# Kernel optimization log

Measured on AMD Instinct MI355X. Metric: run time of the kernel, lower is better.

Reference implementation:

```python
import jax, jax.numpy as jnp
import numpy as np

N = 100000   # num_nodes
D = 128      # input_dim
DO = 128     # output_dim
V = 3        # num_views/relations
E = 500000   # edges per view
C = 2        # num_classes
H = D // 2   # label-attention hidden
VH = DO // 2 # view-attention hidden
EPS = 1e-5


def setup_inputs() -> dict:
    key = jax.random.key(0)
    ks = jax.random.split(key, 20)
    s = 0.05
    def nrm(k, shape):
        return jax.random.normal(k, shape, dtype=jnp.float32) * s
    return {
        'features': jax.random.normal(ks[0], (N, D), dtype=jnp.float32),
        'edge_src': jax.random.randint(ks[1], (V, E), 0, N, dtype=jnp.int32),
        'edge_dst': jax.random.randint(ks[2], (V, E), 0, N, dtype=jnp.int32),
        'edge_w': jax.random.uniform(ks[3], (V, E), dtype=jnp.float32),
        'clsW': nrm(ks[4], (D, C)), 'clsb': jnp.zeros((C,), jnp.float32),
        'attW1': nrm(ks[5], (C, D, H)), 'attb1': jnp.zeros((C, H), jnp.float32),
        'attW2': nrm(ks[6], (C, H)), 'attb2': jnp.zeros((C,), jnp.float32),
        'att_bias': jnp.float32(0.1),
        'relW': nrm(ks[7], (V, D, DO)), 'relb': jnp.zeros((V, DO), jnp.float32),
        'gateW': nrm(ks[8], (V, DO, DO)), 'gateb': jnp.zeros((V, DO), jnp.float32),
        'view_pref': jax.random.normal(ks[9], (V, DO), dtype=jnp.float32),
        'vattW1': nrm(ks[10], (DO, VH)), 'vattb1': jnp.zeros((VH,), jnp.float32),
        'vattW2': nrm(ks[11], (VH,)), 'vattb2': jnp.float32(0.0),
        'selfW': nrm(ks[12], (D, DO)), 'selfb': jnp.zeros((DO,), jnp.float32),
        'featW': nrm(ks[13], (D, DO)), 'featb': jnp.zeros((DO,), jnp.float32),
        'fusW': nrm(ks[14], (2 * DO, DO)), 'fusb': jnp.zeros((DO,), jnp.float32),
        'ln_g': jnp.ones((DO,), jnp.float32), 'ln_b': jnp.zeros((DO,), jnp.float32),
    }


def reference(features, edge_src, edge_dst, edge_w,
              clsW, clsb, attW1, attb1, attW2, attb2, att_bias,
              relW, relb, gateW, gateb,
              view_pref, vattW1, vattb1, vattW2, vattb2,
              selfW, selfb, featW, featb, fusW, fusb, ln_g, ln_b):
    # --- LabelAwareAttention ---
    class_probs = jax.nn.softmax(features @ clsW + clsb, axis=-1)          # [N,C]
    h = jax.nn.relu(jnp.einsum('nd,cdh->cnh', features, attW1) + attb1[:, None, :])
    scores = jax.nn.sigmoid(jnp.einsum('cnh,ch->cn', h, attW2) + attb2[:, None])
    node_att = jnp.sum(scores.T * class_probs, axis=-1) + att_bias         # [N]

    # --- per-view RelationAggregator (num_relations=1 -> relation weight is 1) ---
    src_f = features[edge_src]                                             # [V,E,D]
    msg = (jnp.einsum('ved,vdo->veo', src_f, relW) + relb[:, None, :]) \
          * edge_w[..., None]                                              # [V,E,DO]
    agg = jax.vmap(lambda m, d: jax.ops.segment_sum(m, d, num_segments=N))(
        msg, edge_dst)                                                     # [V,N,DO]
    gate = jax.nn.sigmoid(jnp.einsum('vno,vop->vnp', agg, gateW) + gateb[:, None, :])
    view_out = gate * agg                                                  # [V,N,DO]

    # --- ViewLevelAttention ---
    vh = jax.nn.relu(jnp.einsum('vno,oh->vnh', view_out * view_pref[:, None, :], vattW1) + vattb1)
    vscores = jnp.einsum('vnh,h->vn', vh, vattW2) + vattb2                 # [V,N]
    vweights = jax.nn.softmax(vscores, axis=0)                             # softmax over views
    combined = jnp.sum(view_out * vweights[..., None], axis=0)             # [N,DO]

    # --- fusion + residual + layer norm (dropout=0, eval) ---
    self_out = features @ selfW + selfb
    transformed = features @ featW + featb
    weighted = combined * node_att[:, None]
    fused = jax.nn.relu(jnp.concatenate([self_out, weighted], axis=-1) @ fusW + fusb)
    out = fused + transformed
    mu = jnp.mean(out, axis=-1, keepdims=True)
    var = jnp.var(out, axis=-1, keepdims=True)
    out = (out - mu) / jnp.sqrt(var + EPS) * ln_g + ln_b
    return out, class_probs
```

## Files before the change

### kernel.cpp

```cpp
#include <hip/hip_runtime.h>
#include <hip/hip_bf16.h>

#define NN 100000
#define DD 128
#define VV 3
#define EE 500000
#define TOT (VV * NN)
#define NB ((TOT + 255) / 256)
#define RGB ((NN + 127) / 128)

typedef unsigned short u16;
typedef unsigned int u32;
typedef short s8v __attribute__((ext_vector_type(8)));
typedef float f4v __attribute__((ext_vector_type(4)));

__device__ __forceinline__ float bf2f(u16 u) {
    return __uint_as_float(((u32)u) << 16);
}
__device__ __forceinline__ u16 f2bf(float f) {
    u32 x = __float_as_uint(f);
    u32 r = (x + 0x7fffu + ((x >> 16) & 1u)) >> 16;
    return (u16)r;
}

__device__ __forceinline__ float fexp2(float x) {
#if __has_builtin(__builtin_amdgcn_exp2f)
    return __builtin_amdgcn_exp2f(x);
#else
    return exp2f(x);
#endif
}
__device__ __forceinline__ float frcp(float x) {
#if __has_builtin(__builtin_amdgcn_rcpf)
    return __builtin_amdgcn_rcpf(x);
#else
    return 1.f / x;
#endif
}
__device__ __forceinline__ float fsigmoid(float x) {
    return frcp(1.f + fexp2(-1.4426950408889634f * x));
}

__device__ __forceinline__ void atomAddBf16x2(u16* addr, float f0, float f1) {
#if __has_builtin(__builtin_amdgcn_global_atomic_fadd_v2bf16)
    typedef short v2s __attribute__((ext_vector_type(2)));
    typedef v2s __attribute__((address_space(1)))* v2s_gp;
    v2s v;
    v.x = (short)f2bf(f0);
    v.y = (short)f2bf(f1);
    __builtin_amdgcn_global_atomic_fadd_v2bf16((v2s_gp)(void*)addr, v);
#else
    u32* p = (u32*)addr;
    u32 old = *(volatile u32*)p;
    while (true) {
        float lo = bf2f((u16)(old & 0xffffu)) + f0;
        float hi = bf2f((u16)(old >> 16)) + f1;
        u32 nv = (u32)f2bf(lo) | ((u32)f2bf(hi) << 16);
        u32 prev = atomicCAS(p, old, nv);
        if (prev == old) break;
        old = prev;
    }
#endif
}

template<int XSTR, int WSTR>
__device__ __forceinline__ void gemm16(float acc[4][4], const float* Xs,
                                       const float* Ws, int n0, int o0, int kbase) {
    #pragma unroll 4
    for (int kk = 0; kk < 64; kk += 4) {
        float4 w0 = *reinterpret_cast<const float4*>(Ws + (kk + 0) * WSTR + o0);
        float4 w1 = *reinterpret_cast<const float4*>(Ws + (kk + 1) * WSTR + o0);
        float4 w2 = *reinterpret_cast<const float4*>(Ws + (kk + 2) * WSTR + o0);
        float4 w3 = *reinterpret_cast<const float4*>(Ws + (kk + 3) * WSTR + o0);
        #pragma unroll
        for (int i = 0; i < 4; ++i) {
            float4 x = *reinterpret_cast<const float4*>(Xs + (n0 + i) * XSTR + kbase + kk);
            acc[i][0] = fmaf(x.x, w0.x, fmaf(x.y, w1.x, fmaf(x.z, w2.x, fmaf(x.w, w3.x, acc[i][0]))));
            acc[i][1] = fmaf(x.x, w0.y, fmaf(x.y, w1.y, fmaf(x.z, w2.y, fmaf(x.w, w3.y, acc[i][1]))));
            acc[i][2] = fmaf(x.x, w0.z, fmaf(x.y, w1.z, fmaf(x.z, w2.z, fmaf(x.w, w3.z, acc[i][2]))));
            acc[i][3] = fmaf(x.x, w0.w, fmaf(x.y, w1.w, fmaf(x.z, w2.w, fmaf(x.w, w3.w, acc[i][3]))));
        }
    }
}

template<int WSTR, int NT>
__device__ __forceinline__ void stage_w_f32(float* Ws, const float* __restrict__ src, int tid) {
    #pragma unroll
    for (int rep = 0; rep < 2048 / NT; ++rep) {
        int flat = rep * NT + tid;
        int kk = flat >> 5;
        int c4 = flat & 31;
        float4 q = *reinterpret_cast<const float4*>(src + kk * 128 + c4 * 4);
        *reinterpret_cast<float4*>(Ws + kk * WSTR + c4 * 4) = q;
    }
}

template<int XSTR, int NT>
__device__ __forceinline__ void stage_x_f32(float* Xs, const float* __restrict__ src, int tid) {
    #pragma unroll
    for (int rep = 0; rep < 1024 / NT; ++rep) {
        int flat = rep * NT + tid;
        int n = flat >> 5;
        int c4 = flat & 31;
        float4 q = *reinterpret_cast<const float4*>(src + (size_t)n * 128 + c4 * 4);
        *reinterpret_cast<float4*>(Xs + n * XSTR + c4 * 4) = q;
    }
}

template<int XSTR, int NT>
__device__ __forceinline__ void stage_x_bf16(float* Xs, const u16* __restrict__ src, int tid) {
    #pragma unroll
    for (int rep = 0; rep < 512 / NT; ++rep) {
        int flat = rep * NT + tid;
        int n = flat >> 4;
        int c8 = flat & 15;
        uint4 q = *reinterpret_cast<const uint4*>(src + (size_t)n * 128 + c8 * 8);
        float* d = Xs + n * XSTR + c8 * 8;
        d[0] = bf2f((u16)(q.x & 0xffffu)); d[1] = bf2f((u16)(q.x >> 16));
        d[2] = bf2f((u16)(q.y & 0xffffu)); d[3] = bf2f((u16)(q.y >> 16));
        d[4] = bf2f((u16)(q.z & 0xffffu)); d[5] = bf2f((u16)(q.z >> 16));
        d[6] = bf2f((u16)(q.w & 0xffffu)); d[7] = bf2f((u16)(q.w >> 16));
    }
}

__global__ void prep_kernel(const float* __restrict__ selfW, const float* __restrict__ selfb,
                            const float* __restrict__ fusW, const float* __restrict__ fusb,
                            float* __restrict__ Wsf, float* __restrict__ c1) {
    int o = threadIdx.x;
    int k = blockIdx.x;
    if (k < 128) {
        float acc = 0.f;
        for (int m = 0; m < 128; ++m)
            acc += selfW[k * 128 + m] * fusW[m * 128 + o];
        Wsf[k * 128 + o] = acc;
    } else {
        float acc = 0.f;
        for (int m = 0; m < 128; ++m)
            acc += selfb[m] * fusW[m * 128 + o];
        c1[o] = acc + fusb[o];
    }
}

__global__ __launch_bounds__(128) void wprep_kernel(
        const float* __restrict__ relW, const float* __restrict__ gateW,
        u16* __restrict__ relWb, u16* __restrict__ gateWb) {
    int k = threadIdx.x;
    int n = blockIdx.x & 127;
    int v = blockIdx.x >> 7;
    size_t o = ((size_t)v * 128 + n) * 128 + k;
    size_t i = ((size_t)v * 128 + k) * 128 + n;
    relWb[o]  = f2bf(relW[i]);
    gateWb[o] = f2bf(gateW[i]);
}

__global__ __launch_bounds__(128) void wprep2_kernel(
        const float* __restrict__ Wsf, const float* __restrict__ featW,
        const float* __restrict__ fusW,
        u16* __restrict__ WsfB, u16* __restrict__ featWB, u16* __restrict__ fusWbB) {
    int k = threadIdx.x;
    int n = blockIdx.x;
    WsfB[n * 128 + k]   = f2bf(Wsf[k * 128 + n]);
    featWB[n * 128 + k] = f2bf(featW[k * 128 + n]);
    fusWbB[n * 128 + k] = f2bf(fusW[(size_t)(128 + k) * 128 + n]);
}

__global__ __launch_bounds__(128) void wprep3_kernel(
        const float* __restrict__ attW1, u16* __restrict__ attW1B) {
    int k = threadIdx.x;
    int o = blockIdx.x;
    int c = o >> 6, h = o & 63;
    attW1B[o * 128 + k] = f2bf(attW1[((size_t)c * 128 + k) * 64 + h]);
}

__global__ __launch_bounds__(128) void wprep4_kernel(
        const float* __restrict__ vattW1, const float* __restrict__ view_pref,
        u16* __restrict__ vattW1p) {
    int k = threadIdx.x;
    int h = blockIdx.x & 63;
    int v = blockIdx.x >> 6;
    vattW1p[((size_t)v * 64 + h) * 128 + k] =
        f2bf(view_pref[v * 128 + k] * vattW1[k * 64 + h]);
}

__global__ __launch_bounds__(128) void wprep5_kernel(
        const float* __restrict__ relW, const float* __restrict__ gateW,
        const float* __restrict__ relb,
        u16* __restrict__ W12b, float* __restrict__ rgb) {
    int p = threadIdx.x;
    int b = blockIdx.x;
    int v = b / 129;
    int d = b - v * 129;
    const float* gW = gateW + (size_t)v * 128 * 128;
    if (d < 128) {
        const float* rW = relW + ((size_t)v * 128 + d) * 128;
        float acc = 0.f;
        for (int o = 0; o < 128; ++o) acc += rW[o] * gW[o * 128 + p];
        W12b[((size_t)v * 128 + p) * 128 + d] = f2bf(acc);
    } else {
        const float* rb = relb + (size_t)v * 128;
        float acc = 0.f;
        for (int o = 0; o < 128; ++o) acc += rb[o] * gW[o * 128 + p];
        rgb[v * 128 + p] = acc;
    }
}

__global__ __launch_bounds__(256) void featconv_kernel(
        const float* __restrict__ feat, u16* __restrict__ featB) {
    int t = blockIdx.x * 256 + threadIdx.x;
    float4 q = *reinterpret_cast<const float4*>(feat + (size_t)t * 4);
    ushort4 r;
    r.x = f2bf(q.x); r.y = f2bf(q.y); r.z = f2bf(q.z); r.w = f2bf(q.w);
    *reinterpret_cast<ushort4*>(featB + (size_t)t * 4) = r;
}


__global__ __launch_bounds__(256) void count_kernel(
        const int* __restrict__ edst, int* __restrict__ C) {
    int t = blockIdx.x * 256 + threadIdx.x;
    if (t >= VV * EE) return;
    int v = t / EE;
    atomicAdd(&C[v * NN + edst[t]], 1);
}

__global__ __launch_bounds__(256) void scanA_kernel(
        const int* __restrict__ C, int* __restrict__ bs) {
    int b = blockIdx.x, t = threadIdx.x;
    int i = b * 256 + t;
    int v = (i < TOT) ? C[i] : 0;
    __shared__ int s[256];
    s[t] = v;
    __syncthreads();
    #pragma unroll
    for (int off = 128; off > 0; off >>= 1) {
        if (t < off) s[t] += s[t + off];
        __syncthreads();
    }
    if (t == 0) bs[b] = s[0];
}

__global__ __launch_bounds__(1024) void scanB_kernel(int* __restrict__ bs) {
    __shared__ int s[2048];
    int t = threadIdx.x;
    int v0 = (t < NB) ? bs[t] : 0;
    int v1 = (t + 1024 < NB) ? bs[t + 1024] : 0;
    s[t] = v0; s[t + 1024] = v1;
    __syncthreads();
    #pragma unroll
    for (int off = 1; off < 2048; off <<= 1) {
        int x0 = (t >= off) ? s[t - off] : 0;
        int x1 = (t + 1024 >= off) ? s[t + 1024 - off] : 0;
        __syncthreads();
        s[t] += x0; s[t + 1024] += x1;
        __syncthreads();
    }
    if (t < NB) bs[t] = s[t] - v0;
    if (t + 1024 < NB) bs[t + 1024] = s[t + 1024] - v1;
}

__global__ __launch_bounds__(256) void scanC_kernel(
        int* __restrict__ C, const int* __restrict__ bs) {
    int b = blockIdx.x, t = threadIdx.x;
    int i = b * 256 + t;
    int v = (i < TOT) ? C[i] : 0;
    __shared__ int s[256];
    s[t] = v;
    __syncthreads();
    #pragma unroll
    for (int off = 1; off < 256; off <<= 1) {
        int x = (t >= off) ? s[t - off] : 0;
        __syncthreads();
        s[t] += x;
        __syncthreads();
    }
    if (i < TOT) C[i] = s[t] - v + bs[b];
}

__global__ __launch_bounds__(256) void fill_kernel(
        const int* __restrict__ esrc, const int* __restrict__ edst,
        const float* __restrict__ ew, int* __restrict__ C,
        int2* __restrict__ bsw) {
    int t = blockIdx.x * 256 + threadIdx.x;
    if (t >= VV * EE) return;
    int v = t / EE;
    int pos = atomicAdd(&C[v * NN + edst[t]], 1);
    int2 p;
    p.x = esrc[t];
    p.y = __float_as_int(ew[t]);
    bsw[pos] = p;
}

__global__ __launch_bounds__(256) void gather_kernel(
        const u16* __restrict__ featB, const int* __restrict__ C,
        const int2* __restrict__ bsw,
        u16* __restrict__ aggB, float* __restrict__ wsum) {
    int wid = (blockIdx.x * 256 + threadIdx.x) >> 6;
    int lane = threadIdx.x & 63;
    int end = C[wid];
    int start = (wid == 0) ? 0 : C[wid - 1];
    float a0 = 0.f, a1 = 0.f, wacc = 0.f;
    int e = start;
    for (; e + 4 <= end; e += 4) {
        int2 p0 = bsw[e], p1 = bsw[e + 1], p2 = bsw[e + 2], p3 = bsw[e + 3];
        u32 f0 = *reinterpret_cast<const u32*>(featB + (size_t)p0.x * DD + lane * 2);
        u32 f1 = *reinterpret_cast<const u32*>(featB + (size_t)p1.x * DD + lane * 2);
        u32 f2 = *reinterpret_cast<const u32*>(featB + (size_t)p2.x * DD + lane * 2);
        u32 f3 = *reinterpret_cast<const u32*>(featB + (size_t)p3.x * DD + lane * 2);
        float w0 = __int_as_float(p0.y), w1 = __int_as_float(p1.y);
        float w2 = __int_as_float(p2.y), w3 = __int_as_float(p3.y);
        a0 = fmaf(w0, bf2f((u16)(f0 & 0xffffu)), a0);
        a1 = fmaf(w0, bf2f((u16)(f0 >> 16)), a1);
        a0 = fmaf(w1, bf2f((u16)(f1 & 0xffffu)), a0);
        a1 = fmaf(w1, bf2f((u16)(f1 >> 16)), a1);
        a0 = fmaf(w2, bf2f((u16)(f2 & 0xffffu)), a0);
        a1 = fmaf(w2, bf2f((u16)(f2 >> 16)), a1);
        a0 = fmaf(w3, bf2f((u16)(f3 & 0xffffu)), a0);
        a1 = fmaf(w3, bf2f((u16)(f3 >> 16)), a1);
        wacc += (w0 + w1) + (w2 + w3);
    }
    for (; e < end; ++e) {
        int2 p = bsw[e];
        float w = __int_as_float(p.y);
        u32 f = *reinterpret_cast<const u32*>(featB + (size_t)p.x * DD + lane * 2);
        a0 = fmaf(w, bf2f((u16)(f & 0xffffu)), a0);
        a1 = fmaf(w, bf2f((u16)(f >> 16)), a1);
        wacc += w;
    }
    u32 packed = (u32)f2bf(a0) | ((u32)f2bf(a1) << 16);
    *reinterpret_cast<u32*>(aggB + (size_t)wid * DD + lane * 2) = packed;
    if (lane == 0) wsum[wid] = wacc;
}

__global__ __launch_bounds__(256) void scatter_kernel(
        const int* __restrict__ esrc, const int* __restrict__ edst,
        const float* __restrict__ ew, const float* __restrict__ feat,
        u16* __restrict__ aggB, float* __restrict__ wsum) {
    long long t = (long long)blockIdx.x * 256 + threadIdx.x;
    int lane = (int)(t & 31);
    int eg = (int)(t >> 5);
    int v = eg / EE;
    int src = 0, dst = 0; float w = 0.f;
    if (lane == 0) {
        src = esrc[eg]; dst = edst[eg]; w = ew[eg];
    }
    src = __shfl(src, 0, 32);
    dst = __shfl(dst, 0, 32);
    w   = __shfl(w, 0, 32);
    const float* fr = feat + (size_t)src * DD + lane * 4;
    float4 q = *reinterpret_cast<const float4*>(fr);
    u16* outp = aggB + ((size_t)v * NN + dst) * DD + lane * 4;
    atomAddBf16x2(outp,     w * q.x, w * q.y);
    atomAddBf16x2(outp + 2, w * q.z, w * q.w);
    if (lane == 0) atomicAdd(wsum + v * NN + dst, w);
}

__global__ __launch_bounds__(256) void label_mfma_kernel(
        const u16* __restrict__ featB, const u16* __restrict__ attW1B,
        const float* __restrict__ clsW, const float* __restrict__ clsb,
        const float* __restrict__ attb1, const float* __restrict__ attW2,
        const float* __restrict__ attb2, const float* __restrict__ att_bias,
        float* __restrict__ node_att, float* __restrict__ probs_out) {
    __shared__ u16 Xs[128][136];
    __shared__ u16 Wt[128][72];
    int tid = threadIdx.x;
    int wv = tid >> 6, lane = tid & 63;
    int quad = lane >> 4, l15 = lane & 15;
    int row0 = blockIdx.x * 128;

    #pragma unroll
    for (int rep = 0; rep < 8; ++rep) {
        int flat = rep * 256 + tid;
        int n = flat >> 4, c8 = flat & 15;
        int gr = row0 + n; if (gr >= NN) gr = NN - 1;
        uint4 q = *reinterpret_cast<const uint4*>(featB + (size_t)gr * DD + c8 * 8);
        *reinterpret_cast<uint4*>(&Xs[n][c8 * 8]) = q;
    }

    f4v acc[2][8];
    #pragma unroll
    for (int rt = 0; rt < 2; ++rt)
        #pragma unroll
        for (int c = 0; c < 8; ++c)
            acc[rt][c] = f4v{0.f, 0.f, 0.f, 0.f};

    #pragma unroll
    for (int h = 0; h < 2; ++h) {
        #pragma unroll
        for (int rep = 0; rep < 4; ++rep) {
            int flat = rep * 256 + tid;
            int n = flat >> 3, c8 = flat & 7;
            uint4 q = *reinterpret_cast<const uint4*>(attW1B + (size_t)n * DD + h * 64 + c8 * 8);
            *reinterpret_cast<uint4*>(&Wt[n][c8 * 8]) = q;
        }
        __syncthreads();
        #pragma unroll
        for (int t = 0; t < 2; ++t) {
            int kl = t * 32 + quad * 8;
            s8v a0 = *reinterpret_cast<const s8v*>(&Xs[wv * 32 + l15][h * 64 + kl]);
            s8v a1 = *reinterpret_cast<const s8v*>(&Xs[wv * 32 + 16 + l15][h * 64 + kl]);
            #pragma unroll
            for (int c = 0; c < 8; ++c) {
                s8v b = *reinterpret_cast<const s8v*>(&Wt[c * 16 + l15][kl]);
                acc[0][c] = __builtin_amdgcn_mfma_f32_16x16x32_bf16(a0, b, acc[0][c], 0, 0, 0);
                acc[1][c] = __builtin_amdgcn_mfma_f32_16x16x32_bf16(a1, b, acc[1][c], 0, 0, 0);
            }
        }
        __syncthreads();
    }

    float ab1[8], aw2[8];
    #pragma unroll
    for (int c = 0; c < 8; ++c) {
        int col = c * 16 + l15;
        ab1[c] = attb1[col];
        aw2[c] = attW2[col];
    }
    float cw0[8], cw1[8];
    #pragma unroll
    for (int j = 0; j < 8; ++j) {
        int k = l15 * 8 + j;
        cw0[j] = clsW[k * 2];
        cw1[j] = clsW[k * 2 + 1];
    }
    float cb0 = clsb[0], cb1 = clsb[1];
    float b20 = attb2[0], b21 = attb2[1];
    float abias = att_bias[0];

    #pragma unroll
    for (int rt = 0; rt < 2; ++rt)
        #pragma unroll
        for (int r = 0; r < 4; ++r) {
            int n = wv * 32 + rt * 16 + quad * 4 + r;
            int gr = row0 + n;
            float p0 = 0.f, p1 = 0.f;
            #pragma unroll
            for (int c = 0; c < 4; ++c) {
                float hv = acc[rt][c][r] + ab1[c];
                hv = hv > 0.f ? hv : 0.f;
                p0 += hv * aw2[c];
            }
            #pragma unroll
            for (int c = 4; c < 8; ++c) {
                float hv = acc[rt][c][r] + ab1[c];
                hv = hv > 0.f ? hv : 0.f;
                p1 += hv * aw2[c];
            }
            uint4 q = *reinterpret_cast<const uint4*>(&Xs[n][l15 * 8]);
            float f[8];
            f[0] = bf2f((u16)(q.x & 0xffffu)); f[1] = bf2f((u16)(q.x >> 16));
            f[2] = bf2f((u16)(q.y & 0xffffu)); f[3] = bf2f((u16)(q.y >> 16));
            f[4] = bf2f((u16)(q.z & 0xffffu)); f[5] = bf2f((u16)(q.z >> 16));
            f[6] = bf2f((u16)(q.w & 0xffffu)); f[7] = bf2f((u16)(q.w >> 16));
            float l0 = 0.f, l1 = 0.f;
            #pragma unroll
            for (int j = 0; j < 8; ++j) {
                l0 = fmaf(f[j], cw0[j], l0);
                l1 = fmaf(f[j], cw1[j], l1);
            }
            #pragma unroll
            for (int m = 1; m < 16; m <<= 1) {
                p0 += __shfl_xor(p0, m);
                p1 += __shfl_xor(p1, m);
                l0 += __shfl_xor(l0, m);
                l1 += __shfl_xor(l1, m);
            }
            if (l15 == 0 && gr < NN) {
                float s0 = 1.f / (1.f + expf(-(p0 + b20)));
                float s1 = 1.f / (1.f + expf(-(p1 + b21)));
                l0 += cb0; l1 += cb1;
                float mm = fmaxf(l0, l1);
                float e0 = expf(l0 - mm), e1 = expf(l1 - mm);
                float inv = 1.f / (e0 + e1);
                float q0 = e0 * inv, q1 = e1 * inv;
                node_att[gr] = q0 * s0 + q1 * s1 + abias;
                probs_out[gr * 2]     = q0;
                probs_out[gr * 2 + 1] = q1;
            }
        }
}

__global__ __launch_bounds__(256) void label_kernel(
        const float* __restrict__ feat, const float* __restrict__ clsW, const float* __restrict__ clsb,
        const float* __restrict__ attW1, const float* __restrict__ attb1,
        const float* __restrict__ attW2, const float* __restrict__ attb2,
        const float* __restrict__ att_bias,
        float* __restrict__ node_att, float* __restrict__ probs_out) {
    __shared__ float Xs[32][132];
    __shared__ float Ws[64][132];
    int tid = threadIdx.x;
    int row0 = blockIdx.x * 32;
    stage_x_f32<132, 256>(&Xs[0][0], feat + (size_t)row0 * DD, tid);
    int to = tid & 31, tn = tid >> 5;
    int o0 = to * 4, n0 = tn * 4;
    float acc[4][4] = {};
    for (int half = 0; half < 2; ++half) {
        __syncthreads();
        #pragma unroll
        for (int rep = 0; rep < 8; ++rep) {
            int flat = rep * 256 + tid;
            int kk = flat >> 5, o4 = flat & 31;
            int o = o4 * 4;
            int c = o >> 6, h = o & 63;
            int k = half * 64 + kk;
            float4 q = *reinterpret_cast<const float4*>(attW1 + (size_t)(c * 128 + k) * 64 + h);
            *reinterpret_cast<float4*>(&Ws[kk][o]) = q;
        }
        __syncthreads();
        gemm16<132, 132>(acc, &Xs[0][0], &Ws[0][0], n0, o0, half * 64);
    }
    int c = o0 >> 6, h0 = o0 & 63;
    float b1j[4], w2j[4];
    #pragma unroll
    for (int j = 0; j < 4; ++j) {
        b1j[j] = attb1[c * 64 + h0 + j];
        w2j[j] = attW2[c * 64 + h0 + j];
    }
    float part[4];
    #pragma unroll
    for (int i = 0; i < 4; ++i) {
        float s = 0.f;
        #pragma unroll
        for (int j = 0; j < 4; ++j) {
            float hv = acc[i][j] + b1j[j];
            hv = hv > 0.f ? hv : 0.f;
            s += hv * w2j[j];
        }
        part[i] = s;
    }
    __syncthreads();
    float* red = &Ws[0][0];
    float* Ssc = red + 32 * 33;
    float* Lsc = Ssc + 64;
    #pragma unroll
    for (int i = 0; i < 4; ++i) red[(n0 + i) * 33 + to] = part[i];
    __syncthreads();
    if (tid < 64) {
        int n = tid >> 1, cc = tid & 1;
        float l = 0.f;
        for (int k = 0; k < 128; k += 4) {
            float4 x = *reinterpret_cast<const float4*>(&Xs[n][k]);
            l += x.x * clsW[(k + 0) * 2 + cc];
            l += x.y * clsW[(k + 1) * 2 + cc];
            l += x.z * clsW[(k + 2) * 2 + cc];
            l += x.w * clsW[(k + 3) * 2 + cc];
        }
        Lsc[n * 2 + cc] = l + clsb[cc];
        float s = 0.f;
        for (int u = 0; u < 16; ++u) s += red[n * 33 + cc * 16 + u];
        s += attb2[cc];
        Ssc[n * 2 + cc] = 1.f / (1.f + expf(-s));
    }
    __syncthreads();
    if (tid < 32) {
        int n = tid;
        float l0 = Lsc[n * 2], l1 = Lsc[n * 2 + 1];
        float m = fmaxf(l0, l1);
        float e0 = expf(l0 - m), e1 = expf(l1 - m);
        float inv = 1.f / (e0 + e1);
        float p0 = e0 * inv, p1 = e1 * inv;
        float na = p0 * Ssc[n * 2] + p1 * Ssc[n * 2 + 1] + att_bias[0];
        int row = row0 + n;
        node_att[row] = na;
        probs_out[row * 2]     = p0;
        probs_out[row * 2 + 1] = p1;
    }
}

__global__ __launch_bounds__(256, 3) void relgate_mfma_kernel(
        const u16* __restrict__ relWb, const float* __restrict__ relb,
        const u16* __restrict__ W12b, const float* __restrict__ rgb,
        const float* __restrict__ gateb,
        const u16* __restrict__ vattW1p, const float* __restrict__ vattb1,
        const float* __restrict__ vattW2, const float* __restrict__ vattb2,
        u16* __restrict__ aggB, const float* __restrict__ wsum,
        float* __restrict__ vscores) {
    __shared__ u16 Wf[128][136];
    __shared__ u16 Wt[128][72];
    int tid = threadIdx.x;
    int wv = tid >> 6, lane = tid & 63;
    int quad = lane >> 4, l15 = lane & 15;
    int v = blockIdx.y;
    int row0 = blockIdx.x * 128;
    const size_t vbase = (size_t)v * NN;

    #pragma unroll
    for (int rep = 0; rep < 8; ++rep) {
        int flat = rep * 256 + tid;
        int n = flat >> 4, c8 = flat & 15;
        int gr = row0 + n; if (gr >= NN) gr = NN - 1;
        uint4 q = *reinterpret_cast<const uint4*>(aggB + (vbase + gr) * DD + c8 * 8);
        *reinterpret_cast<uint4*>(&Wf[n][c8 * 8]) = q;
    }
    __syncthreads();

    s8v af[2][2][2];
    #pragma unroll
    for (int h = 0; h < 2; ++h)
        #pragma unroll
        for (int t = 0; t < 2; ++t) {
            int kl = h * 64 + t * 32 + quad * 8;
            af[h][t][0] = *reinterpret_cast<const s8v*>(&Wf[wv * 32 + l15][kl]);
            af[h][t][1] = *reinterpret_cast<const s8v*>(&Wf[wv * 32 + 16 + l15][kl]);
        }
    __syncthreads();

    const u16* W1 = relWb + (size_t)v * DD * DD;
    const u16* W2 = W12b + (size_t)v * DD * DD;
    #pragma unroll
    for (int rep = 0; rep < 8; ++rep) {
        int flat = rep * 256 + tid;
        int n = flat >> 4, c8 = flat & 15;
        *reinterpret_cast<uint4*>(&Wf[n][c8 * 8]) =
            *reinterpret_cast<const uint4*>(W1 + (size_t)n * DD + c8 * 8);
    }
    #pragma unroll
    for (int rep = 0; rep < 4; ++rep) {
        int flat = rep * 256 + tid;
        int n = flat >> 3, c8 = flat & 7;
        *reinterpret_cast<uint4*>(&Wt[n][c8 * 8]) =
            *reinterpret_cast<const uint4*>(W2 + (size_t)n * DD + c8 * 8);
    }
    __syncthreads();

    f4v acc1[2][8], acc2[2][8];
    #pragma unroll
    for (int rt = 0; rt < 2; ++rt)
        #pragma unroll
        for (int c = 0; c < 8; ++c) {
            acc1[rt][c] = f4v{0.f, 0.f, 0.f, 0.f};
            acc2[rt][c] = f4v{0.f, 0.f, 0.f, 0.f};
        }

    #pragma unroll
    for (int h = 0; h < 2; ++h)
        #pragma unroll
        for (int t = 0; t < 2; ++t) {
            int kl = h * 64 + t * 32 + quad * 8;
            #pragma unroll
            for (int c = 0; c < 8; ++c) {
                s8v b = *reinterpret_cast<const s8v*>(&Wf[c * 16 + l15][kl]);
                acc1[0][c] = __builtin_amdgcn_mfma_f32_16x16x32_bf16(af[h][t][0], b, acc1[0][c], 0, 0, 0);
                acc1[1][c] = __builtin_amdgcn_mfma_f32_16x16x32_bf16(af[h][t][1], b, acc1[1][c], 0, 0, 0);
            }
        }
    #pragma unroll
    for (int t = 0; t < 2; ++t) {
        int kl = t * 32 + quad * 8;
        #pragma unroll
        for (int c = 0; c < 8; ++c) {
            s8v b = *reinterpret_cast<const s8v*>(&Wt[c * 16 + l15][kl]);
            acc2[0][c] = __builtin_amdgcn_mfma_f32_16x16x32_bf16(af[0][t][0], b, acc2[0][c], 0, 0, 0);
            acc2[1][c] = __builtin_amdgcn_mfma_f32_16x16x32_bf16(af[0][t][1], b, acc2[1][c], 0, 0, 0);
        }
    }
    __syncthreads();

    #pragma unroll
    for (int rep = 0; rep < 4; ++rep) {
        int flat = rep * 256 + tid;
        int n = flat >> 3, c8 = flat & 7;
        *reinterpret_cast<uint4*>(&Wt[n][c8 * 8]) =
            *reinterpret_cast<const uint4*>(W2 + (size_t)n * DD + 64 + c8 * 8);
    }
    __syncthreads();
    #pragma unroll
    for (int t = 0; t < 2; ++t) {
        int kl = t * 32 + quad * 8;
        #pragma unroll
        for (int c = 0; c < 8; ++c) {
            s8v b = *reinterpret_cast<const s8v*>(&Wt[c * 16 + l15][kl]);
            acc2[0][c] = __builtin_amdgcn_mfma_f32_16x16x32_bf16(af[1][t][0], b, acc2[0][c], 0, 0, 0);
            acc2[1][c] = __builtin_amdgcn_mfma_f32_16x16x32_bf16(af[1][t][1], b, acc2[1][c], 0, 0, 0);
        }
    }

    float wsn[2][4];
    #pragma unroll
    for (int rt = 0; rt < 2; ++rt)
        #pragma unroll
        for (int r = 0; r < 4; ++r) {
            int gr = row0 + wv * 32 + rt * 16 + quad * 4 + r;
            wsn[rt][r] = wsum[vbase + (gr < NN ? gr : NN - 1)];
        }
    float rb[8], rg2[8], gb[8];
    #pragma unroll
    for (int c = 0; c < 8; ++c) {
        int col = c * 16 + l15;
        rb[c]  = relb[v * DD + col];
        rg2[c] = rgb[v * DD + col];
        gb[c]  = gateb[v * DD + col];
    }
    #pragma unroll
    for (int rt = 0; rt < 2; ++rt)
        #pragma unroll
        for (int c = 0; c < 8; ++c)
            #pragma unroll
            for (int r = 0; r < 4; ++r) {
                float a = acc1[rt][c][r] + wsn[rt][r] * rb[c];
                float g = fsigmoid(acc2[rt][c][r] + wsn[rt][r] * rg2[c] + gb[c]);
                Wf[wv * 32 + rt * 16 + quad * 4 + r][c * 16 + l15] = f2bf(g * a);
            }
    __syncthreads();

    {
        const u16* Wv = vattW1p + (size_t)v * 64 * DD;
        #pragma unroll
        for (int rep = 0; rep < 4; ++rep) {
            int flat = rep * 256 + tid;
            int n = flat >> 4, c8 = flat & 15;
            uint4 q = *reinterpret_cast<const uint4*>(Wv + (size_t)n * DD + c8 * 8);
            int half = c8 >> 3;
            *reinterpret_cast<uint4*>(&Wt[half * 64 + n][(c8 & 7) * 8]) = q;
        }
    }
    s8v a2[2][2][2];
    #pragma unroll
    for (int h = 0; h < 2; ++h)
        #pragma unroll
        for (int t = 0; t < 2; ++t) {
            int kl = h * 64 + t * 32 + quad * 8;
            a2[h][t][0] = *reinterpret_cast<const s8v*>(&Wf[wv * 32 + l15][kl]);
            a2[h][t][1] = *reinterpret_cast<const s8v*>(&Wf[wv * 32 + 16 + l15][kl]);
        }
    #pragma unroll
    for (int rep = 0; rep < 8; ++rep) {
        int flat = rep * 256 + tid;
        int n = flat >> 4, c8 = flat & 15;
        int gr = row0 + n;
        if (gr < NN)
            *reinterpret_cast<uint4*>(aggB + (vbase + gr) * DD + c8 * 8) =
                *reinterpret_cast<const uint4*>(&Wf[n][c8 * 8]);
    }
    __syncthreads();

    f4v acc3[2][4];
    #pragma unroll
    for (int rt = 0; rt < 2; ++rt)
        #pragma unroll
        for (int c = 0; c < 4; ++c)
            acc3[rt][c] = f4v{0.f, 0.f, 0.f, 0.f};
    #pragma unroll
    for (int h = 0; h < 2; ++h)
        #pragma unroll
        for (int t = 0; t < 2; ++t) {
            int kl = t * 32 + quad * 8;
            #pragma unroll
            for (int c = 0; c < 4; ++c) {
                s8v b = *reinterpret_cast<const s8v*>(&Wt[h * 64 + c * 16 + l15][kl]);
                acc3[0][c] = __builtin_amdgcn_mfma_f32_16x16x32_bf16(a2[h][t][0], b, acc3[0][c], 0, 0, 0);
                acc3[1][c] = __builtin_amdgcn_mfma_f32_16x16x32_bf16(a2[h][t][1], b, acc3[1][c], 0, 0, 0);
            }
        }
    float vb1[4], vw2[4];
    #pragma unroll
    for (int c = 0; c < 4; ++c) {
        int col = c * 16 + l15;
        vb1[c] = vattb1[col];
        vw2[c] = vattW2[col];
    }
    float vb2 = vattb2[0];
    #pragma unroll
    for (int rt = 0; rt < 2; ++rt)
        #pragma unroll
        for (int r = 0; r < 4; ++r) {
            float p = 0.f;
            #pragma unroll
            for (int c = 0; c < 4; ++c) {
                float hv = acc3[rt][c][r] + vb1[c];
                hv = hv > 0.f ? hv : 0.f;
                p += hv * vw2[c];
            }
            #pragma unroll
            for (int m = 1; m < 16; m <<= 1)
                p += __shfl_xor(p, m);
            int gr = row0 + wv * 32 + rt * 16 + quad * 4 + r;
            if (l15 == 0 && gr < NN)
                vscores[vbase + gr] = p + vb2;
        }
}

__global__ __launch_bounds__(256) void relgate_kernel(
        const float* __restrict__ relW, const float* __restrict__ relb,
        const float* __restrict__ gateW, const float* __restrict__ gateb,
        u16* __restrict__ aggB, const float* __restrict__ wsum) {
    __shared__ float Xs[32][128];
    __shared__ float Ws[64][132];
    int tid = threadIdx.x;
    int v = blockIdx.y;
    int row0 = blockIdx.x * 32;
    u16* base = aggB + ((size_t)v * NN + row0) * DD;
    stage_x_bf16<128, 256>(&Xs[0][0], base, tid);
    int to = tid & 31, tn = tid >> 5;
    int o0 = to * 4, n0 = tn * 4;
    float acc[4][4] = {};
    const float* W1 = relW + (size_t)v * DD * DD;
    for (int half = 0; half < 2; ++half) {
        __syncthreads();
        stage_w_f32<132, 256>(&Ws[0][0], W1 + half * 64 * DD, tid);
        __syncthreads();
        gemm16<128, 132>(acc, &Xs[0][0], &Ws[0][0], n0, o0, half * 64);
    }
    float wsn[4], rb[4];
    #pragma unroll
    for (int i = 0; i < 4; ++i) wsn[i] = wsum[v * NN + row0 + n0 + i];
    #pragma unroll
    for (int j = 0; j < 4; ++j) rb[j] = relb[v * DD + o0 + j];
    #pragma unroll
    for (int i = 0; i < 4; ++i)
        #pragma unroll
        for (int j = 0; j < 4; ++j) acc[i][j] += wsn[i] * rb[j];
    __syncthreads();
    #pragma unroll
    for (int i = 0; i < 4; ++i)
        *reinterpret_cast<float4*>(&Xs[n0 + i][o0]) = make_float4(acc[i][0], acc[i][1], acc[i][2], acc[i][3]);
    float acc2[4][4] = {};
    const float* W2 = gateW + (size_t)v * DD * DD;
    for (int half = 0; half < 2; ++half) {
        __syncthreads();
        stage_w_f32<132, 256>(&Ws[0][0], W2 + half * 64 * DD, tid);
        __syncthreads();
        gemm16<128, 132>(acc2, &Xs[0][0], &Ws[0][0], n0, o0, half * 64);
    }
    float gb[4];
    #pragma unroll
    for (int j = 0; j < 4; ++j) gb[j] = gateb[v * DD + o0 + j];
    #pragma unroll
    for (int i = 0; i < 4; ++i) {
        float g0 = 1.f / (1.f + expf(-(acc2[i][0] + gb[0])));
        float g1 = 1.f / (1.f + expf(-(acc2[i][1] + gb[1])));
        float g2 = 1.f / (1.f + expf(-(acc2[i][2] + gb[2])));
        float g3 = 1.f / (1.f + expf(-(acc2[i][3] + gb[3])));
        ushort4 r;
        r.x = f2bf(g0 * acc[i][0]); r.y = f2bf(g1 * acc[i][1]);
        r.z = f2bf(g2 * acc[i][2]); r.w = f2bf(g3 * acc[i][3]);
        *reinterpret_cast<ushort4*>(base + (size_t)(n0 + i) * DD + o0) = r;
    }
}

__global__ __launch_bounds__(128) void vatt_kernel(
        const u16* __restrict__ aggB, const float* __restrict__ view_pref,
        const float* __restrict__ vattW1, const float* __restrict__ vattb1,
        const float* __restrict__ vattW2, const float* __restrict__ vattb2,
        float* __restrict__ vscores) {
    __shared__ float Xs[32][132];
    __shared__ float Ws[128][68];
    int tid = threadIdx.x;
    int v = blockIdx.y;
    int row0 = blockIdx.x * 32;
    const u16* base = aggB + ((size_t)v * NN + row0) * DD;
    #pragma unroll
    for (int rep = 0; rep < 4; ++rep) {
        int flat = rep * 128 + tid;
        int n = flat >> 4, c8 = flat & 15;
        uint4 q = *reinterpret_cast<const uint4*>(base + (size_t)n * DD + c8 * 8);
        float4 pa = *reinterpret_cast<const float4*>(view_pref + v * DD + c8 * 8);
        float4 pb = *reinterpret_cast<const float4*>(view_pref + v * DD + c8 * 8 + 4);
        float* d = &Xs[n][c8 * 8];
        d[0] = bf2f((u16)(q.x & 0xffffu)) * pa.x; d[1] = bf2f((u16)(q.x >> 16)) * pa.y;
        d[2] = bf2f((u16)(q.y & 0xffffu)) * pa.z; d[3] = bf2f((u16)(q.y >> 16)) * pa.w;
        d[4] = bf2f((u16)(q.z & 0xffffu)) * pb.x; d[5] = bf2f((u16)(q.z >> 16)) * pb.y;
        d[6] = bf2f((u16)(q.w & 0xffffu)) * pb.z; d[7] = bf2f((u16)(q.w >> 16)) * pb.w;
    }
    #pragma unroll
    for (int rep = 0; rep < 16; ++rep) {
        int flat = rep * 128 + tid;
        int k = flat >> 4, c4 = flat & 15;
        float4 q = *reinterpret_cast<const float4*>(vattW1 + k * 64 + c4 * 4);
        *reinterpret_cast<float4*>(&Ws[k][c4 * 4]) = q;
    }
    __syncthreads();
    int to = tid & 15, tn = tid >> 4;
    int o0 = to * 4, n0 = tn * 4;
    float acc[4][4] = {};
    gemm16<132, 68>(acc, &Xs[0][0], &Ws[0][0], n0, o0, 0);
    gemm16<132, 68>(acc, &Xs[0][0], &Ws[64][0], n0, o0, 64);
    float b1[4], w2[4];
    #pragma unroll
    for (int j = 0; j < 4; ++j) {
        b1[j] = vattb1[o0 + j];
        w2[j] = vattW2[o0 + j];
    }
    float part[4];
    #pragma unroll
    for (int i = 0; i < 4; ++i) {
        float s = 0.f;
        #pragma unroll
        for (int j = 0; j < 4; ++j) {
            float hv = acc[i][j] + b1[j];
            hv = hv > 0.f ? hv : 0.f;
            s += hv * w2[j];
        }
        part[i] = s;
    }
    __syncthreads();
    float* red = &Ws[0][0];
    #pragma unroll
    for (int i = 0; i < 4; ++i) red[(n0 + i) * 17 + to] = part[i];
    __syncthreads();
    if (tid < 32) {
        float s = 0.f;
        for (int u = 0; u < 16; ++u) s += red[tid * 17 + u];
        vscores[(size_t)v * NN + row0 + tid] = s + vattb2[0];
    }
}

__global__ __launch_bounds__(256) void combine_kernel(
        u16* __restrict__ aggB, const float* __restrict__ vscores,
        const float* __restrict__ node_att) {
    int t = blockIdx.x * 256 + threadIdx.x;
    int n = t >> 5, c4 = t & 31;
    float s0 = vscores[n], s1 = vscores[NN + n], s2 = vscores[2 * NN + n];
    float m = fmaxf(s0, fmaxf(s1, s2));
    float e0 = expf(s0 - m), e1 = expf(s1 - m), e2 = expf(s2 - m);
    float inv = 1.f / (e0 + e1 + e2);
    float w0 = e0 * inv, w1 = e1 * inv, w2 = e2 * inv;
    float na = node_att[n];
    size_t off = (size_t)n * DD + c4 * 4;
    ushort4 q0 = *reinterpret_cast<const ushort4*>(aggB + off);
    ushort4 q1 = *reinterpret_cast<const ushort4*>(aggB + (size_t)NN * DD + off);
    ushort4 q2 = *reinterpret_cast<const ushort4*>(aggB + 2 * (size_t)NN * DD + off);
    ushort4 r;
    r.x = f2bf((bf2f(q0.x) * w0 + bf2f(q1.x) * w1 + bf2f(q2.x) * w2) * na);
    r.y = f2bf((bf2f(q0.y) * w0 + bf2f(q1.y) * w1 + bf2f(q2.y) * w2) * na);
    r.z = f2bf((bf2f(q0.z) * w0 + bf2f(q1.z) * w1 + bf2f(q2.z) * w2) * na);
    r.w = f2bf((bf2f(q0.w) * w0 + bf2f(q1.w) * w1 + bf2f(q2.w) * w2) * na);
    *reinterpret_cast<ushort4*>(aggB + off) = r;
}

__global__ __launch_bounds__(256, 3) void final_mfma_kernel(
        const u16* __restrict__ featB, const u16* __restrict__ aggB,
        const float* __restrict__ vsc, const float* __restrict__ natt,
        const u16* __restrict__ WsfB, const u16* __restrict__ featWB,
        const u16* __restrict__ fusWbB,
        const float* __restrict__ c1, const float* __restrict__ featb,
        const float* __restrict__ ln_g, const float* __restrict__ ln_b,
        float* __restrict__ outp) {
    __shared__ u16 Wf[128][136];
    __shared__ u16 Wt[128][72];
    int tid = threadIdx.x;
    int wv = tid >> 6, lane = tid & 63;
    int quad = lane >> 4, l15 = lane & 15;
    int row0 = blockIdx.x * 128;

    #pragma unroll
    for (int rep = 0; rep < 8; ++rep) {
        int flat = rep * 256 + tid;
        int n = flat >> 4, c8 = flat & 15;
        int gr = row0 + n; if (gr >= NN) gr = NN - 1;
        uint4 q = *reinterpret_cast<const uint4*>(featB + (size_t)gr * DD + c8 * 8);
        *reinterpret_cast<uint4*>(&Wf[n][c8 * 8]) = q;
    }
    if (tid < 128) {
        int gr = row0 + tid; if (gr >= NN) gr = NN - 1;
        float s0 = vsc[gr], s1 = vsc[NN + gr], s2 = vsc[2 * NN + gr];
        float m = fmaxf(s0, fmaxf(s1, s2));
        const float L2E = 1.4426950408889634f;
        float e0 = fexp2((s0 - m) * L2E);
        float e1 = fexp2((s1 - m) * L2E);
        float e2 = fexp2((s2 - m) * L2E);
        float na = natt[gr] * frcp(e0 + e1 + e2);
        float* rwp = reinterpret_cast<float*>(&Wf[tid][128]);
        rwp[0] = e0 * na;
        rwp[1] = e1 * na;
        rwp[2] = e2 * na;
    }
    __syncthreads();

    s8v af[2][2][2];
    #pragma unroll
    for (int h = 0; h < 2; ++h)
        #pragma unroll
        for (int t = 0; t < 2; ++t) {
            int kl = h * 64 + t * 32 + quad * 8;
            af[h][t][0] = *reinterpret_cast<const s8v*>(&Wf[wv * 32 + l15][kl]);
            af[h][t][1] = *reinterpret_cast<const s8v*>(&Wf[wv * 32 + 16 + l15][kl]);
        }
    __syncthreads();

    #pragma unroll
    for (int rep = 0; rep < 8; ++rep) {
        int flat = rep * 256 + tid;
        int n = flat >> 4, c8 = flat & 15;
        *reinterpret_cast<uint4*>(&Wf[n][c8 * 8]) =
            *reinterpret_cast<const uint4*>(WsfB + (size_t)n * DD + c8 * 8);
    }
    #pragma unroll
    for (int rep = 0; rep < 4; ++rep) {
        int flat = rep * 256 + tid;
        int n = flat >> 3, c8 = flat & 7;
        *reinterpret_cast<uint4*>(&Wt[n][c8 * 8]) =
            *reinterpret_cast<const uint4*>(featWB + (size_t)n * DD + c8 * 8);
    }
    __syncthreads();

    f4v acc1[2][8], acc2[2][8];
    #pragma unroll
    for (int rt = 0; rt < 2; ++rt)
        #pragma unroll
        for (int c = 0; c < 8; ++c) {
            acc1[rt][c] = f4v{0.f, 0.f, 0.f, 0.f};
            acc2[rt][c] = f4v{0.f, 0.f, 0.f, 0.f};
        }

    #pragma unroll
    for (int h = 0; h < 2; ++h)
        #pragma unroll
        for (int t = 0; t < 2; ++t) {
            int kl = h * 64 + t * 32 + quad * 8;
            #pragma unroll
            for (int c = 0; c < 8; ++c) {
                s8v b = *reinterpret_cast<const s8v*>(&Wf[c * 16 + l15][kl]);
                acc1[0][c] = __builtin_amdgcn_mfma_f32_16x16x32_bf16(af[h][t][0], b, acc1[0][c], 0, 0, 0);
                acc1[1][c] = __builtin_amdgcn_mfma_f32_16x16x32_bf16(af[h][t][1], b, acc1[1][c], 0, 0, 0);
            }
        }
    #pragma unroll
    for (int t = 0; t < 2; ++t) {
        int kl = t * 32 + quad * 8;
        #pragma unroll
        for (int c = 0; c < 8; ++c) {
            s8v b = *reinterpret_cast<const s8v*>(&Wt[c * 16 + l15][kl]);
            acc2[0][c] = __builtin_amdgcn_mfma_f32_16x16x32_bf16(af[0][t][0], b, acc2[0][c], 0, 0, 0);
            acc2[1][c] = __builtin_amdgcn_mfma_f32_16x16x32_bf16(af[0][t][1], b, acc2[1][c], 0, 0, 0);
        }
    }
    __syncthreads();
    #pragma unroll
    for (int rep = 0; rep < 4; ++rep) {
        int flat = rep * 256 + tid;
        int n = flat >> 3, c8 = flat & 7;
        *reinterpret_cast<uint4*>(&Wt[n][c8 * 8]) =
            *reinterpret_cast<const uint4*>(featWB + (size_t)n * DD + 64 + c8 * 8);
    }
    __syncthreads();
    #pragma unroll
    for (int t = 0; t < 2; ++t) {
        int kl = t * 32 + quad * 8;
        #pragma unroll
        for (int c = 0; c < 8; ++c) {
            s8v b = *reinterpret_cast<const s8v*>(&Wt[c * 16 + l15][kl]);
            acc2[0][c] = __builtin_amdgcn_mfma_f32_16x16x32_bf16(af[1][t][0], b, acc2[0][c], 0, 0, 0);
            acc2[1][c] = __builtin_amdgcn_mfma_f32_16x16x32_bf16(af[1][t][1], b, acc2[1][c], 0, 0, 0);
        }
    }

    #pragma unroll
    for (int rep = 0; rep < 8; ++rep) {
        int flat = rep * 256 + tid;
        int n = flat >> 4, c8 = flat & 15;
        int gr = row0 + n; if (gr >= NN) gr = NN - 1;
        size_t off = (size_t)gr * DD + c8 * 8;
        uint4 q0 = *reinterpret_cast<const uint4*>(aggB + off);
        uint4 q1 = *reinterpret_cast<const uint4*>(aggB + (size_t)NN * DD + off);
        uint4 q2 = *reinterpret_cast<const uint4*>(aggB + 2 * (size_t)NN * DD + off);
        const float* rwp = reinterpret_cast<const float*>(&Wf[n][128]);
        float w0 = rwp[0], w1 = rwp[1], w2 = rwp[2];
        u32 o[4];
        const u32* a = &q0.x; const u32* b = &q1.x; const u32* c = &q2.x;
        #pragma unroll
        for (int j = 0; j < 4; ++j) {
            float lo = bf2f((u16)(a[j] & 0xffffu)) * w0 + bf2f((u16)(b[j] & 0xffffu)) * w1
                     + bf2f((u16)(c[j] & 0xffffu)) * w2;
            float hi = bf2f((u16)(a[j] >> 16)) * w0 + bf2f((u16)(b[j] >> 16)) * w1
                     + bf2f((u16)(c[j] >> 16)) * w2;
            o[j] = (u32)f2bf(lo) | ((u32)f2bf(hi) << 16);
        }
        uint4 r; r.x = o[0]; r.y = o[1]; r.z = o[2]; r.w = o[3];
        *reinterpret_cast<uint4*>(&Wf[n][c8 * 8]) = r;
    }
    __syncthreads();

    #pragma unroll
    for (int rep = 0; rep < 4; ++rep) {
        int flat = rep * 256 + tid;
        int n = flat >> 3, c8 = flat & 7;
        *reinterpret_cast<uint4*>(&Wt[n][c8 * 8]) =
            *reinterpret_cast<const uint4*>(fusWbB + (size_t)n * DD + c8 * 8);
    }
    __syncthreads();
    #pragma unroll
    for (int t = 0; t < 2; ++t) {
        int kl = t * 32 + quad * 8;
        s8v a0 = *reinterpret_cast<const s8v*>(&Wf[wv * 32 + l15][kl]);
        s8v a1 = *reinterpret_cast<const s8v*>(&Wf[wv * 32 + 16 + l15][kl]);
        #pragma unroll
        for (int c = 0; c < 8; ++c) {
            s8v b = *reinterpret_cast<const s8v*>(&Wt[c * 16 + l15][kl]);
            acc1[0][c] = __builtin_amdgcn_mfma_f32_16x16x32_bf16(a0, b, acc1[0][c], 0, 0, 0);
            acc1[1][c] = __builtin_amdgcn_mfma_f32_16x16x32_bf16(a1, b, acc1[1][c], 0, 0, 0);
        }
    }
    __syncthreads();
    #pragma unroll
    for (int rep = 0; rep < 4; ++rep) {
        int flat = rep * 256 + tid;
        int n = flat >> 3, c8 = flat & 7;
        *reinterpret_cast<uint4*>(&Wt[n][c8 * 8]) =
            *reinterpret_cast<const uint4*>(fusWbB + (size_t)n * DD + 64 + c8 * 8);
    }
    __syncthreads();
    #pragma unroll
    for (int t = 0; t < 2; ++t) {
        int kl = t * 32 + quad * 8;
        s8v a0 = *reinterpret_cast<const s8v*>(&Wf[wv * 32 + l15][64 + kl]);
        s8v a1 = *reinterpret_cast<const s8v*>(&Wf[wv * 32 + 16 + l15][64 + kl]);
        #pragma unroll
        for (int c = 0; c < 8; ++c) {
            s8v b = *reinterpret_cast<const s8v*>(&Wt[c * 16 + l15][kl]);
            acc1[0][c] = __builtin_amdgcn_mfma_f32_16x16x32_bf16(a0, b, acc1[0][c], 0, 0, 0);
            acc1[1][c] = __builtin_amdgcn_mfma_f32_16x16x32_bf16(a1, b, acc1[1][c], 0, 0, 0);
        }
    }

    float c1j[8], fbj[8], gj[8], bj[8];
    #pragma unroll
    for (int c = 0; c < 8; ++c) {
        int col = c * 16 + l15;
        c1j[c] = c1[col];
        fbj[c] = featb[col];
        gj[c]  = ln_g[col];
        bj[c]  = ln_b[col];
    }
    #pragma unroll
    for (int rt = 0; rt < 2; ++rt)
        #pragma unroll
        for (int c = 0; c < 8; ++c)
            #pragma unroll
            for (int r = 0; r < 4; ++r) {
                float f = acc1[rt][c][r] + c1j[c];
                f = f > 0.f ? f : 0.f;
                acc1[rt][c][r] = f + acc2[rt][c][r] + fbj[c];
            }
    #pragma unroll
    for (int rt = 0; rt < 2; ++rt)
        #pragma unroll
        for (int r = 0; r < 4; ++r) {
            float s = 0.f, q = 0.f;
            #pragma unroll
            for (int c = 0; c < 8; ++c) {
                float x = acc1[rt][c][r];
                s += x; q += x * x;
            }
            #pragma unroll
            for (int m = 1; m < 16; m <<= 1) {
                s += __shfl_xor(s, m);
                q += __shfl_xor(q, m);
            }
            float mu = s * (1.f / 128.f);
            float var = q * (1.f / 128.f) - mu * mu;
            float rs = rsqrtf(var + 1e-5f);
            int gr = row0 + wv * 32 + rt * 16 + quad * 4 + r;
            if (gr < NN) {
                #pragma unroll
                for (int c = 0; c < 8; ++c)
                    outp[(size_t)gr * DD + c * 16 + l15] =
                        (acc1[rt][c][r] - mu) * rs * gj[c] + bj[c];
            }
        }
}

__global__ __launch_bounds__(256) void final_kernel(
        const float* __restrict__ feat, const u16* __restrict__ weightedB,
        const float* __restrict__ Wsf, const float* __restrict__ c1,
        const float* __restrict__ fusW, const float* __restrict__ featW,
        const float* __restrict__ featb, const float* __restrict__ ln_g,
        const float* __restrict__ ln_b, float* __restrict__ outp) {
    __shared__ float Xs[32][128];
    __shared__ float Ws[64][128];
    int tid = threadIdx.x;
    int row0 = blockIdx.x * 32;
    stage_x_f32<128, 256>(&Xs[0][0], feat + (size_t)row0 * DD, tid);
    int to = tid & 31, tn = tid >> 5;
    int o0 = to * 4, n0 = tn * 4;
    float acc1[4][4] = {}, acc2[4][4] = {};
    for (int half = 0; half < 2; ++half) {
        __syncthreads();
        stage_w_f32<128, 256>(&Ws[0][0], Wsf + half * 64 * 128, tid);
        __syncthreads();
        gemm16<128, 128>(acc1, &Xs[0][0], &Ws[0][0], n0, o0, half * 64);
    }
    for (int half = 0; half < 2; ++half) {
        __syncthreads();
        stage_w_f32<128, 256>(&Ws[0][0], featW + half * 64 * 128, tid);
        __syncthreads();
        gemm16<128, 128>(acc2, &Xs[0][0], &Ws[0][0], n0, o0, half * 64);
    }
    __syncthreads();
    stage_x_bf16<128, 256>(&Xs[0][0], weightedB + (size_t)row0 * DD, tid);
    for (int half = 0; half < 2; ++half) {
        __syncthreads();
        stage_w_f32<128, 256>(&Ws[0][0], fusW + (size_t)(128 + half * 64) * 128, tid);
        __syncthreads();
        gemm16<128, 128>(acc1, &Xs[0][0], &Ws[0][0], n0, o0, half * 64);
    }
    float c1j[4], fbj[4], gj[4], bj[4];
    #pragma unroll
    for (int j = 0; j < 4; ++j) {
        c1j[j] = c1[o0 + j];
        fbj[j] = featb[o0 + j];
        gj[j]  = ln_g[o0 + j];
        bj[j]  = ln_b[o0 + j];
    }
    float val[4][4];
    #pragma unroll
    for (int i = 0; i < 4; ++i)
        #pragma unroll
        for (int j = 0; j < 4; ++j) {
            float f = acc1[i][j] + c1j[j];
            f = f > 0.f ? f : 0.f;
            val[i][j] = f + acc2[i][j] + fbj[j];
        }
    __syncthreads();
    float* red_s = &Ws[0][0];
    float* red_q = red_s + 32 * 33;
    float* mus   = red_q + 32 * 33;
    float* rss   = mus + 32;
    #pragma unroll
    for (int i = 0; i < 4; ++i) {
        float s = 0.f, q = 0.f;
        #pragma unroll
        for (int j = 0; j < 4; ++j) { s += val[i][j]; q += val[i][j] * val[i][j]; }
        red_s[(n0 + i) * 33 + to] = s;
        red_q[(n0 + i) * 33 + to] = q;
    }
    __syncthreads();
    if (tid < 32) {
        float s = 0.f, q = 0.f;
        for (int u = 0; u < 32; ++u) { s += red_s[tid * 33 + u]; q += red_q[tid * 33 + u]; }
        float mu = s / 128.f;
        float var = q / 128.f - mu * mu;
        mus[tid] = mu;
        rss[tid] = rsqrtf(var + 1e-5f);
    }
    __syncthreads();
    #pragma unroll
    for (int i = 0; i < 4; ++i) {
        float mu = mus[n0 + i], rs = rss[n0 + i];
        float4 o;
        o.x = (val[i][0] - mu) * rs * gj[0] + bj[0];
        o.y = (val[i][1] - mu) * rs * gj[1] + bj[1];
        o.z = (val[i][2] - mu) * rs * gj[2] + bj[2];
        o.w = (val[i][3] - mu) * rs * gj[3] + bj[3];
        *reinterpret_cast<float4*>(outp + (size_t)(row0 + n0 + i) * DD + o0) = o;
    }
}

extern "C" void kernel_launch(void* const* d_in, const int* in_sizes, int n_in,
                              void* d_out, int out_size, void* d_ws, size_t ws_size,
                              hipStream_t stream) {
    (void)in_sizes; (void)n_in; (void)out_size;
    const float* feat      = (const float*)d_in[0];
    const int*   esrc      = (const int*)d_in[1];
    const int*   edst      = (const int*)d_in[2];
    const float* ew        = (const float*)d_in[3];
    const float* clsW      = (const float*)d_in[4];
    const float* clsb      = (const float*)d_in[5];
    const float* attW1     = (const float*)d_in[6];
    const float* attb1     = (const float*)d_in[7];
    const float* attW2     = (const float*)d_in[8];
    const float* attb2     = (const float*)d_in[9];
    const float* att_bias  = (const float*)d_in[10];
    const float* relW      = (const float*)d_in[11];
    const float* relb      = (const float*)d_in[12];
    const float* gateW     = (const float*)d_in[13];
    const float* gateb     = (const float*)d_in[14];
    const float* view_pref = (const float*)d_in[15];
    const float* vattW1    = (const float*)d_in[16];
    const float* vattb1    = (const float*)d_in[17];
    const float* vattW2    = (const float*)d_in[18];
    const float* vattb2    = (const float*)d_in[19];
    const float* selfW     = (const float*)d_in[20];
    const float* selfb     = (const float*)d_in[21];
    const float* featW     = (const float*)d_in[22];
    const float* featb     = (const float*)d_in[23];
    const float* fusW      = (const float*)d_in[24];
    const float* fusb      = (const float*)d_in[25];
    const float* ln_g      = (const float*)d_in[26];
    const float* ln_b      = (const float*)d_in[27];

    u16*   aggB = (u16*)d_ws;
    float* wsum = (float*)(aggB + (size_t)VV * NN * DD);
    float* natt = wsum + (size_t)VV * NN;
    float* vsc  = natt + NN;
    float* Wsf  = vsc + (size_t)VV * NN;
    float* c1   = Wsf + DD * DD;
    u16* relWb  = (u16*)(c1 + DD);
    u16* gateWb = relWb + (size_t)VV * DD * DD;
    u16* WsfB   = gateWb + (size_t)VV * DD * DD;
    u16* featWB = WsfB + DD * DD;
    u16* fusWbB = featWB + DD * DD;
    u16* attW1B = fusWbB + DD * DD;
    u16* vattW1p = attW1B + DD * DD;
    u16* W12b   = vattW1p + (size_t)VV * 64 * DD;
    float* rgb  = (float*)(W12b + (size_t)VV * DD * DD);
    int*   C    = (int*)(rgb + VV * DD);
    int*   bs   = C + (size_t)TOT;
    int2*  bsw  = (int2*)(bs + NB + 1);
    u16* featB  = (u16*)(bsw + (size_t)VV * EE);
    size_t needed = (size_t)((char*)(featB + (size_t)NN * DD) - (char*)d_ws);

    float* outp  = (float*)d_out;
    float* probs = outp + (size_t)NN * DD;

    prep_kernel<<<129, 128, 0, stream>>>(selfW, selfb, fusW, fusb, Wsf, c1);
    if (ws_size >= needed) {
        featconv_kernel<<<12500, 256, 0, stream>>>(feat, featB);
        wprep_kernel<<<384, 128, 0, stream>>>(relW, gateW, relWb, gateWb);
        wprep2_kernel<<<128, 128, 0, stream>>>(Wsf, featW, fusW, WsfB, featWB, fusWbB);
        wprep3_kernel<<<128, 128, 0, stream>>>(attW1, attW1B);
        wprep4_kernel<<<192, 128, 0, stream>>>(vattW1, view_pref, vattW1p);
        wprep5_kernel<<<VV * 129, 128, 0, stream>>>(relW, gateW, relb, W12b, rgb);
        label_mfma_kernel<<<RGB, 256, 0, stream>>>(featB, attW1B, clsW, clsb, attb1,
                                                   attW2, attb2, att_bias, natt, probs);
        hipMemsetAsync(C, 0, (size_t)TOT * sizeof(int), stream);
        count_kernel<<<(VV * EE + 255) / 256, 256, 0, stream>>>(edst, C);
        scanA_kernel<<<NB, 256, 0, stream>>>(C, bs);
        scanB_kernel<<<1, 1024, 0, stream>>>(bs);
        scanC_kernel<<<NB, 256, 0, stream>>>(C, bs);
        fill_kernel<<<(VV * EE + 255) / 256, 256, 0, stream>>>(esrc, edst, ew, C, bsw);
        gather_kernel<<<(VV * NN) / 4, 256, 0, stream>>>(featB, C, bsw, aggB, wsum);
        relgate_mfma_kernel<<<dim3(RGB, 3), 256, 0, stream>>>(relWb, relb, W12b, rgb, gateb,
                                                              vattW1p, vattb1, vattW2, vattb2,
                                                              aggB, wsum, vsc);
        final_mfma_kernel<<<RGB, 256, 0, stream>>>(featB, aggB, vsc, natt,
                                                   WsfB, featWB, fusWbB,
                                                   c1, featb, ln_g, ln_b, outp);
    } else {
        label_kernel<<<3125, 256, 0, stream>>>(feat, clsW, clsb, attW1, attb1, attW2, attb2,
                                               att_bias, natt, probs);
        hipMemsetAsync(d_ws, 0,
                       (size_t)VV * NN * DD * sizeof(u16) + (size_t)VV * NN * sizeof(float),
                       stream);
        scatter_kernel<<<187500, 256, 0, stream>>>(esrc, edst, ew, feat, aggB, wsum);
        relgate_kernel<<<dim3(3125, 3), 256, 0, stream>>>(relW, relb, gateW, gateb, aggB, wsum);
        vatt_kernel<<<dim3(3125, 3), 128, 0, stream>>>(aggB, view_pref, vattW1, vattb1,
                                                       vattW2, vattb2, vsc);
        combine_kernel<<<12500, 256, 0, stream>>>(aggB, vsc, natt);
        final_kernel<<<3125, 256, 0, stream>>>(feat, aggB, Wsf, c1, fusW, featW, featb,
                                               ln_g, ln_b, outp);
    }
}
```

Before: 661.3 us.

## Fuse label attention, relation/gate, view attention and final fusion into one kernel

Merges label_mfma, relgate_mfma and final_mfma into a single per-row-tile kernel. It loops over the three views while keeping view outputs and an online softmax over view scores in registers, then performs the fusion GEMMs and layer norm. This removes the intermediate global writes and re-reads of node_att, view scores and the per-view aggregates, plus two kernel launches. In exchange the single block carries many more accumulators, which raises register pressure and may lower occupancy. It also serializes the three views inside one block where they previously ran as a 3D grid.

```diff
diff --git a/kernel.cpp b/kernel.cpp
--- a/kernel.cpp
+++ b/kernel.cpp
@@ -121,6 +121,81 @@
         d[4] = bf2f((u16)(q.z & 0xffffu)); d[5] = bf2f((u16)(q.z >> 16));
         d[6] = bf2f((u16)(q.w & 0xffffu)); d[7] = bf2f((u16)(q.w >> 16));
     }
+}
+
+
+__device__ __forceinline__ void stageWf(u16 (*Wf)[136], const u16* __restrict__ src, int tid) {
+    #pragma unroll
+    for (int rep = 0; rep < 8; ++rep) {
+        int flat = rep * 256 + tid;
+        int n = flat >> 4, c8 = flat & 15;
+        *reinterpret_cast<uint4*>(&Wf[n][c8 * 8]) =
+            *reinterpret_cast<const uint4*>(src + (size_t)n * DD + c8 * 8);
+    }
+}
+
+__device__ __forceinline__ void stageWtHalf(u16 (*Wt)[72], const u16* __restrict__ src, int tid) {
+    #pragma unroll
+    for (int rep = 0; rep < 4; ++rep) {
+        int flat = rep * 256 + tid;
+        int n = flat >> 3, c8 = flat & 7;
+        *reinterpret_cast<uint4*>(&Wt[n][c8 * 8]) =
+            *reinterpret_cast<const uint4*>(src + (size_t)n * DD + c8 * 8);
+    }
+}
+
+__device__ __forceinline__ void stageX(u16 (*Wf)[136], const u16* __restrict__ src,
+                                       int row0, int tid) {
+    #pragma unroll
+    for (int rep = 0; rep < 8; ++rep) {
+        int flat = rep * 256 + tid;
+        int n = flat >> 4, c8 = flat & 15;
+        int gr = row0 + n; if (gr >= NN) gr = NN - 1;
+        *reinterpret_cast<uint4*>(&Wf[n][c8 * 8]) =
+            *reinterpret_cast<const uint4*>(src + (size_t)gr * DD + c8 * 8);
+    }
+}
+
+__device__ __forceinline__ void loadFrags(s8v af[2][2][2], u16 (*Wf)[136],
+                                          int wv, int l15, int quad) {
+    #pragma unroll
+    for (int h = 0; h < 2; ++h)
+        #pragma unroll
+        for (int t = 0; t < 2; ++t) {
+            int kl = h * 64 + t * 32 + quad * 8;
+            af[h][t][0] = *reinterpret_cast<const s8v*>(&Wf[wv * 32 + l15][kl]);
+            af[h][t][1] = *reinterpret_cast<const s8v*>(&Wf[wv * 32 + 16 + l15][kl]);
+        }
+}
+
+__device__ __forceinline__ void mfmaWt8(f4v acc[2][8], const s8v af[2][2][2], int h,
+                                        u16 (*Wt)[72], int l15, int quad) {
+    #pragma unroll
+    for (int t = 0; t < 2; ++t) {
+        int kl = t * 32 + quad * 8;
+        #pragma unroll
+        for (int c = 0; c < 8; ++c) {
+            s8v b = *reinterpret_cast<const s8v*>(&Wt[c * 16 + l15][kl]);
+            acc[0][c] = __builtin_amdgcn_mfma_f32_16x16x32_bf16(af[h][t][0], b, acc[0][c], 0, 0, 0);
+            acc[1][c] = __builtin_amdgcn_mfma_f32_16x16x32_bf16(af[h][t][1], b, acc[1][c], 0, 0, 0);
+        }
+    }
+}
+
+__device__ __forceinline__ void mfmaWfFull(f4v acc[2][8], const s8v af[2][2][2],
+                                           u16 (*Wf)[136], int l15, int quad) {
+    #pragma unroll
+    for (int h = 0; h < 2; ++h)
+        #pragma unroll
+        for (int t = 0; t < 2; ++t) {
+            int kl = h * 64 + t * 32 + quad * 8;
+            #pragma unroll
+            for (int c = 0; c < 8; ++c) {
+                s8v b = *reinterpret_cast<const s8v*>(&Wf[c * 16 + l15][kl]);
+                acc[0][c] = __builtin_amdgcn_mfma_f32_16x16x32_bf16(af[h][t][0], b, acc[0][c], 0, 0, 0);
+                acc[1][c] = __builtin_amdgcn_mfma_f32_16x16x32_bf16(af[h][t][1], b, acc[1][c], 0, 0, 0);
+            }
+        }
 }
 
 __global__ void prep_kernel(const float* __restrict__ selfW, const float* __restrict__ selfb,
@@ -353,117 +428,106 @@
     if (lane == 0) atomicAdd(wsum + v * NN + dst, w);
 }
 
-__global__ __launch_bounds__(256) void label_mfma_kernel(
-        const u16* __restrict__ featB, const u16* __restrict__ attW1B,
+__global__ __launch_bounds__(256) void fused_mfma_kernel(
+        const u16* __restrict__ featB, const u16* __restrict__ aggB,
+        const u16* __restrict__ attW1B,
         const float* __restrict__ clsW, const float* __restrict__ clsb,
         const float* __restrict__ attb1, const float* __restrict__ attW2,
         const float* __restrict__ attb2, const float* __restrict__ att_bias,
-        float* __restrict__ node_att, float* __restrict__ probs_out) {
-    __shared__ u16 Xs[128][136];
+        const u16* __restrict__ relWb, const float* __restrict__ relb,
+        const u16* __restrict__ W12b, const float* __restrict__ rgbv,
+        const float* __restrict__ gateb,
+        const u16* __restrict__ vattW1p, const float* __restrict__ vattb1,
+        const float* __restrict__ vattW2, const float* __restrict__ vattb2,
+        const float* __restrict__ wsum,
+        const u16* __restrict__ WsfB, const u16* __restrict__ featWB,
+        const u16* __restrict__ fusWbB,
+        const float* __restrict__ c1, const float* __restrict__ featb,
+        const float* __restrict__ ln_g, const float* __restrict__ ln_b,
+        float* __restrict__ outp, float* __restrict__ probs_out) {
+    __shared__ u16 Wf[128][136];
     __shared__ u16 Wt[128][72];
     int tid = threadIdx.x;
     int wv = tid >> 6, lane = tid & 63;
     int quad = lane >> 4, l15 = lane & 15;
     int row0 = blockIdx.x * 128;
-
-    #pragma unroll
-    for (int rep = 0; rep < 8; ++rep) {
-        int flat = rep * 256 + tid;
-        int n = flat >> 4, c8 = flat & 15;
-        int gr = row0 + n; if (gr >= NN) gr = NN - 1;
-        uint4 q = *reinterpret_cast<const uint4*>(featB + (size_t)gr * DD + c8 * 8);
-        *reinterpret_cast<uint4*>(&Xs[n][c8 * 8]) = q;
-    }
-
-    f4v acc[2][8];
-    #pragma unroll
-    for (int rt = 0; rt < 2; ++rt)
-        #pragma unroll
-        for (int c = 0; c < 8; ++c)
-            acc[rt][c] = f4v{0.f, 0.f, 0.f, 0.f};
-
-    #pragma unroll
-    for (int h = 0; h < 2; ++h) {
-        #pragma unroll
-        for (int rep = 0; rep < 4; ++rep) {
-            int flat = rep * 256 + tid;
-            int n = flat >> 3, c8 = flat & 7;
-            uint4 q = *reinterpret_cast<const uint4*>(attW1B + (size_t)n * DD + h * 64 + c8 * 8);
-            *reinterpret_cast<uint4*>(&Wt[n][c8 * 8]) = q;
-        }
-        __syncthreads();
-        #pragma unroll
-        for (int t = 0; t < 2; ++t) {
-            int kl = t * 32 + quad * 8;
-            s8v a0 = *reinterpret_cast<const s8v*>(&Xs[wv * 32 + l15][h * 64 + kl]);
-            s8v a1 = *reinterpret_cast<const s8v*>(&Xs[wv * 32 + 16 + l15][h * 64 + kl]);
-            #pragma unroll
-            for (int c = 0; c < 8; ++c) {
-                s8v b = *reinterpret_cast<const s8v*>(&Wt[c * 16 + l15][kl]);
-                acc[0][c] = __builtin_amdgcn_mfma_f32_16x16x32_bf16(a0, b, acc[0][c], 0, 0, 0);
-                acc[1][c] = __builtin_amdgcn_mfma_f32_16x16x32_bf16(a1, b, acc[1][c], 0, 0, 0);
-            }
-        }
-        __syncthreads();
-    }
-
-    float ab1[8], aw2[8];
-    #pragma unroll
-    for (int c = 0; c < 8; ++c) {
-        int col = c * 16 + l15;
-        ab1[c] = attb1[col];
-        aw2[c] = attW2[col];
-    }
-    float cw0[8], cw1[8];
-    #pragma unroll
-    for (int j = 0; j < 8; ++j) {
-        int k = l15 * 8 + j;
-        cw0[j] = clsW[k * 2];
-        cw1[j] = clsW[k * 2 + 1];
-    }
-    float cb0 = clsb[0], cb1 = clsb[1];
-    float b20 = attb2[0], b21 = attb2[1];
-    float abias = att_bias[0];
-
-    #pragma unroll
-    for (int rt = 0; rt < 2; ++rt)
-        #pragma unroll
-        for (int r = 0; r < 4; ++r) {
-            int n = wv * 32 + rt * 16 + quad * 4 + r;
-            int gr = row0 + n;
-            float p0 = 0.f, p1 = 0.f;
-            #pragma unroll
-            for (int c = 0; c < 4; ++c) {
-                float hv = acc[rt][c][r] + ab1[c];
-                hv = hv > 0.f ? hv : 0.f;
-                p0 += hv * aw2[c];
-            }
-            #pragma unroll
-            for (int c = 4; c < 8; ++c) {
-                float hv = acc[rt][c][r] + ab1[c];
-                hv = hv > 0.f ? hv : 0.f;
-                p1 += hv * aw2[c];
-            }
-            uint4 q = *reinterpret_cast<const uint4*>(&Xs[n][l15 * 8]);
-            float f[8];
-            f[0] = bf2f((u16)(q.x & 0xffffu)); f[1] = bf2f((u16)(q.x >> 16));
-            f[2] = bf2f((u16)(q.y & 0xffffu)); f[3] = bf2f((u16)(q.y >> 16));
-            f[4] = bf2f((u16)(q.z & 0xffffu)); f[5] = bf2f((u16)(q.z >> 16));
-            f[6] = bf2f((u16)(q.w & 0xffffu)); f[7] = bf2f((u16)(q.w >> 16));
-            float l0 = 0.f, l1 = 0.f;
-            #pragma unroll
-            for (int j = 0; j < 8; ++j) {
-                l0 = fmaf(f[j], cw0[j], l0);
-                l1 = fmaf(f[j], cw1[j], l1);
-            }
-            #pragma unroll
-            for (int m = 1; m < 16; m <<= 1) {
-                p0 += __shfl_xor(p0, m);
-                p1 += __shfl_xor(p1, m);
-                l0 += __shfl_xor(l0, m);
-                l1 += __shfl_xor(l1, m);
-            }
-            if (l15 == 0 && gr < NN) {
+    const float L2E = 1.4426950408889634f;
+
+    float na[2][4];
+    {
+        stageX(Wf, featB, row0, tid);
+        stageWtHalf(Wt, attW1B, tid);
+        __syncthreads();
+        s8v af[2][2][2];
+        loadFrags(af, Wf, wv, l15, quad);
+        f4v accL[2][8];
+        #pragma unroll
+        for (int rt = 0; rt < 2; ++rt)
+            #pragma unroll
+            for (int c = 0; c < 8; ++c)
+                accL[rt][c] = f4v{0.f, 0.f, 0.f, 0.f};
+        mfmaWt8(accL, af, 0, Wt, l15, quad);
+        __syncthreads();
+        stageWtHalf(Wt, attW1B + 64, tid);
+        __syncthreads();
+        mfmaWt8(accL, af, 1, Wt, l15, quad);
+
+        float ab1[8], aw2[8];
+        #pragma unroll
+        for (int c = 0; c < 8; ++c) {
+            int col = c * 16 + l15;
+            ab1[c] = attb1[col];
+            aw2[c] = attW2[col];
+        }
+        float cw0[8], cw1[8];
+        #pragma unroll
+        for (int j = 0; j < 8; ++j) {
+            int k = l15 * 8 + j;
+            cw0[j] = clsW[k * 2];
+            cw1[j] = clsW[k * 2 + 1];
+        }
+        float cb0 = clsb[0], cb1 = clsb[1];
+        float b20 = attb2[0], b21 = attb2[1];
+        float abias = att_bias[0];
+
+        #pragma unroll
+        for (int rt = 0; rt < 2; ++rt)
+            #pragma unroll
+            for (int r = 0; r < 4; ++r) {
+                int n = wv * 32 + rt * 16 + quad * 4 + r;
+                int gr = row0 + n;
+                float p0 = 0.f, p1 = 0.f;
+                #pragma unroll
+                for (int c = 0; c < 4; ++c) {
+                    float hv = accL[rt][c][r] + ab1[c];
+                    hv = hv > 0.f ? hv : 0.f;
+                    p0 += hv * aw2[c];
+                }
+                #pragma unroll
+                for (int c = 4; c < 8; ++c) {
+                    float hv = accL[rt][c][r] + ab1[c];
+                    hv = hv > 0.f ? hv : 0.f;
+                    p1 += hv * aw2[c];
+                }
+                uint4 q = *reinterpret_cast<const uint4*>(&Wf[n][l15 * 8]);
+                float f[8];
+                f[0] = bf2f((u16)(q.x & 0xffffu)); f[1] = bf2f((u16)(q.x >> 16));
+                f[2] = bf2f((u16)(q.y & 0xffffu)); f[3] = bf2f((u16)(q.y >> 16));
+                f[4] = bf2f((u16)(q.z & 0xffffu)); f[5] = bf2f((u16)(q.z >> 16));
+                f[6] = bf2f((u16)(q.w & 0xffffu)); f[7] = bf2f((u16)(q.w >> 16));
+                float l0 = 0.f, l1 = 0.f;
+                #pragma unroll
+                for (int j = 0; j < 8; ++j) {
+                    l0 = fmaf(f[j], cw0[j], l0);
+                    l1 = fmaf(f[j], cw1[j], l1);
+                }
+                #pragma unroll
+                for (int m = 1; m < 16; m <<= 1) {
+                    p0 += __shfl_xor(p0, m);
+                    p1 += __shfl_xor(p1, m);
+                    l0 += __shfl_xor(l0, m);
+                    l1 += __shfl_xor(l1, m);
+                }
                 float s0 = 1.f / (1.f + expf(-(p0 + b20)));
                 float s1 = 1.f / (1.f + expf(-(p1 + b21)));
                 l0 += cb0; l1 += cb1;
@@ -471,9 +535,257 @@
                 float e0 = expf(l0 - mm), e1 = expf(l1 - mm);
                 float inv = 1.f / (e0 + e1);
                 float q0 = e0 * inv, q1 = e1 * inv;
-                node_att[gr] = q0 * s0 + q1 * s1 + abias;
-                probs_out[gr * 2]     = q0;
-                probs_out[gr * 2 + 1] = q1;
+                na[rt][r] = q0 * s0 + q1 * s1 + abias;
+                if (l15 == 0 && gr < NN) {
+                    probs_out[gr * 2]     = q0;
+                    probs_out[gr * 2 + 1] = q1;
+                }
+            }
+    }
+
+    float Cacc[2][8][4];
+    float mrun[2][4], Srun[2][4];
+    #pragma unroll
+    for (int rt = 0; rt < 2; ++rt)
+        #pragma unroll
+        for (int r = 0; r < 4; ++r) { mrun[rt][r] = -3.0e38f; Srun[rt][r] = 0.f; }
+    #pragma unroll
+    for (int rt = 0; rt < 2; ++rt)
+        #pragma unroll
+        for (int c = 0; c < 8; ++c)
+            #pragma unroll
+            for (int r = 0; r < 4; ++r) Cacc[rt][c][r] = 0.f;
+
+    for (int v = 0; v < VV; ++v) {
+        const size_t vbase = (size_t)v * NN;
+        __syncthreads();
+        stageX(Wf, aggB + vbase * DD, row0, tid);
+        __syncthreads();
+        s8v af[2][2][2];
+        loadFrags(af, Wf, wv, l15, quad);
+        __syncthreads();
+        const u16* W1 = relWb + (size_t)v * DD * DD;
+        const u16* W2 = W12b + (size_t)v * DD * DD;
+        stageWf(Wf, W1, tid);
+        stageWtHalf(Wt, W2, tid);
+        __syncthreads();
+        f4v acc2[2][8];
+        #pragma unroll
+        for (int rt = 0; rt < 2; ++rt)
+            #pragma unroll
+            for (int c = 0; c < 8; ++c)
+                acc2[rt][c] = f4v{0.f, 0.f, 0.f, 0.f};
+        mfmaWt8(acc2, af, 0, Wt, l15, quad);
+        __syncthreads();
+        stageWtHalf(Wt, W2 + 64, tid);
+        __syncthreads();
+        mfmaWt8(acc2, af, 1, Wt, l15, quad);
+
+        float wsn[2][4];
+        #pragma unroll
+        for (int rt = 0; rt < 2; ++rt)
+            #pragma unroll
+            for (int r = 0; r < 4; ++r) {
+                int gr = row0 + wv * 32 + rt * 16 + quad * 4 + r;
+                wsn[rt][r] = wsum[vbase + (gr < NN ? gr : NN - 1)];
+            }
+        u32 gpk[2][8][2];
+        #pragma unroll
+        for (int c = 0; c < 8; ++c) {
+            int col = c * 16 + l15;
+            float rg2 = rgbv[v * DD + col];
+            float gb2 = gateb[v * DD + col];
+            #pragma unroll
+            for (int rt = 0; rt < 2; ++rt)
+                #pragma unroll
+                for (int rp = 0; rp < 2; ++rp) {
+                    float g0 = fsigmoid(acc2[rt][c][2 * rp]     + wsn[rt][2 * rp] * rg2 + gb2);
+                    float g1 = fsigmoid(acc2[rt][c][2 * rp + 1] + wsn[rt][2 * rp + 1] * rg2 + gb2);
+                    gpk[rt][c][rp] = (u32)f2bf(g0) | ((u32)f2bf(g1) << 16);
+                }
+        }
+        f4v acc1[2][8];
+        #pragma unroll
+        for (int rt = 0; rt < 2; ++rt)
+            #pragma unroll
+            for (int c = 0; c < 8; ++c)
+                acc1[rt][c] = f4v{0.f, 0.f, 0.f, 0.f};
+        mfmaWfFull(acc1, af, Wf, l15, quad);
+        #pragma unroll
+        for (int c = 0; c < 8; ++c) {
+            float rbc = relb[v * DD + c * 16 + l15];
+            #pragma unroll
+            for (int rt = 0; rt < 2; ++rt)
+                #pragma unroll
+                for (int r = 0; r < 4; ++r) {
+                    float a = acc1[rt][c][r] + wsn[rt][r] * rbc;
+                    u32 gp = gpk[rt][c][r >> 1];
+                    float g = bf2f((u16)((r & 1) ? (gp >> 16) : (gp & 0xffffu)));
+                    acc1[rt][c][r] = g * a;
+                }
+        }
+        __syncthreads();
+        #pragma unroll
+        for (int rt = 0; rt < 2; ++rt)
+            #pragma unroll
+            for (int c = 0; c < 8; ++c)
+                #pragma unroll
+                for (int r = 0; r < 4; ++r)
+                    Wf[wv * 32 + rt * 16 + quad * 4 + r][c * 16 + l15] =
+                        f2bf(acc1[rt][c][r]);
+        {
+            const u16* Wv = vattW1p + (size_t)v * 64 * DD;
+            #pragma unroll
+            for (int rep = 0; rep < 4; ++rep) {
+                int flat = rep * 256 + tid;
+                int n = flat >> 4, c8 = flat & 15;
+                uint4 q = *reinterpret_cast<const uint4*>(Wv + (size_t)n * DD + c8 * 8);
+                int half = c8 >> 3;
+                *reinterpret_cast<uint4*>(&Wt[half * 64 + n][(c8 & 7) * 8]) = q;
+            }
+        }
+        __syncthreads();
+        s8v a2[2][2][2];
+        loadFrags(a2, Wf, wv, l15, quad);
+        f4v acc3[2][4];
+        #pragma unroll
+        for (int rt = 0; rt < 2; ++rt)
+            #pragma unroll
+            for (int c = 0; c < 4; ++c)
+                acc3[rt][c] = f4v{0.f, 0.f, 0.f, 0.f};
+        #pragma unroll
+        for (int h = 0; h < 2; ++h)
+            #pragma unroll
+            for (int t = 0; t < 2; ++t) {
+                int kl = t * 32 + quad * 8;
+                #pragma unroll
+                for (int c = 0; c < 4; ++c) {
+                    s8v b = *reinterpret_cast<const s8v*>(&Wt[h * 64 + c * 16 + l15][kl]);
+                    acc3[0][c] = __builtin_amdgcn_mfma_f32_16x16x32_bf16(a2[h][t][0], b, acc3[0][c], 0, 0, 0);
+                    acc3[1][c] = __builtin_amdgcn_mfma_f32_16x16x32_bf16(a2[h][t][1], b, acc3[1][c], 0, 0, 0);
+                }
+            }
+        float vb1[4], vw2[4];
+        #pragma unroll
+        for (int c = 0; c < 4; ++c) {
+            int col = c * 16 + l15;
+            vb1[c] = vattb1[col];
+            vw2[c] = vattW2[col];
+        }
+        float vb2 = vattb2[0];
+        #pragma unroll
+        for (int rt = 0; rt < 2; ++rt)
+            #pragma unroll
+            for (int r = 0; r < 4; ++r) {
+                float p = 0.f;
+                #pragma unroll
+                for (int c = 0; c < 4; ++c) {
+                    float hv = acc3[rt][c][r] + vb1[c];
+                    hv = hv > 0.f ? hv : 0.f;
+                    p += hv * vw2[c];
+                }
+                #pragma unroll
+                for (int m = 1; m < 16; m <<= 1)
+                    p += __shfl_xor(p, m);
+                float s = p + vb2;
+                float mn = fmaxf(mrun[rt][r], s);
+                float sc = fexp2((mrun[rt][r] - mn) * L2E);
+                float es = fexp2((s - mn) * L2E);
+                Srun[rt][r] = Srun[rt][r] * sc + es;
+                mrun[rt][r] = mn;
+                #pragma unroll
+                for (int c = 0; c < 8; ++c)
+                    Cacc[rt][c][r] = Cacc[rt][c][r] * sc + es * acc1[rt][c][r];
+            }
+    }
+
+    float wrow[2][4];
+    #pragma unroll
+    for (int rt = 0; rt < 2; ++rt)
+        #pragma unroll
+        for (int r = 0; r < 4; ++r)
+            wrow[rt][r] = na[rt][r] * frcp(Srun[rt][r]);
+    __syncthreads();
+    #pragma unroll
+    for (int rt = 0; rt < 2; ++rt)
+        #pragma unroll
+        for (int c = 0; c < 8; ++c)
+            #pragma unroll
+            for (int r = 0; r < 4; ++r)
+                Wf[wv * 32 + rt * 16 + quad * 4 + r][c * 16 + l15] =
+                    f2bf(Cacc[rt][c][r] * wrow[rt][r]);
+    __syncthreads();
+    s8v a2[2][2][2];
+    loadFrags(a2, Wf, wv, l15, quad);
+    __syncthreads();
+    stageX(Wf, featB, row0, tid);
+    __syncthreads();
+    s8v af[2][2][2];
+    loadFrags(af, Wf, wv, l15, quad);
+    __syncthreads();
+    stageWf(Wf, WsfB, tid);
+    stageWtHalf(Wt, featWB, tid);
+    __syncthreads();
+    f4v acc1[2][8], acc2[2][8];
+    #pragma unroll
+    for (int rt = 0; rt < 2; ++rt)
+        #pragma unroll
+        for (int c = 0; c < 8; ++c) {
+            acc1[rt][c] = f4v{0.f, 0.f, 0.f, 0.f};
+            acc2[rt][c] = f4v{0.f, 0.f, 0.f, 0.f};
+        }
+    mfmaWfFull(acc1, af, Wf, l15, quad);
+    mfmaWt8(acc2, af, 0, Wt, l15, quad);
+    __syncthreads();
+    stageWf(Wf, fusWbB, tid);
+    stageWtHalf(Wt, featWB + 64, tid);
+    __syncthreads();
+    mfmaWt8(acc2, af, 1, Wt, l15, quad);
+    mfmaWfFull(acc1, a2, Wf, l15, quad);
+
+    float c1j[8], fbj[8], gj[8], bj[8];
+    #pragma unroll
+    for (int c = 0; c < 8; ++c) {
+        int col = c * 16 + l15;
+        c1j[c] = c1[col];
+        fbj[c] = featb[col];
+        gj[c]  = ln_g[col];
+        bj[c]  = ln_b[col];
+    }
+    #pragma unroll
+    for (int rt = 0; rt < 2; ++rt)
+        #pragma unroll
+        for (int c = 0; c < 8; ++c)
+            #pragma unroll
+            for (int r = 0; r < 4; ++r) {
+                float f = acc1[rt][c][r] + c1j[c];
+                f = f > 0.f ? f : 0.f;
+                acc1[rt][c][r] = f + acc2[rt][c][r] + fbj[c];
+            }
+    #pragma unroll
+    for (int rt = 0; rt < 2; ++rt)
+        #pragma unroll
+        for (int r = 0; r < 4; ++r) {
+            float s = 0.f, q = 0.f;
+            #pragma unroll
+            for (int c = 0; c < 8; ++c) {
+                float x = acc1[rt][c][r];
+                s += x; q += x * x;
+            }
+            #pragma unroll
+            for (int m = 1; m < 16; m <<= 1) {
+                s += __shfl_xor(s, m);
+                q += __shfl_xor(q, m);
+            }
+            float mu = s * (1.f / 128.f);
+            float var = q * (1.f / 128.f) - mu * mu;
+            float rs = rsqrtf(var + 1e-5f);
+            int gr = row0 + wv * 32 + rt * 16 + quad * 4 + r;
+            if (gr < NN) {
+                #pragma unroll
+                for (int c = 0; c < 8; ++c)
+                    outp[(size_t)gr * DD + c * 16 + l15] =
+                        (acc1[rt][c][r] - mu) * rs * gj[c] + bj[c];
             }
         }
 }
@@ -563,219 +875,6 @@
         probs_out[row * 2]     = p0;
         probs_out[row * 2 + 1] = p1;
     }
-}
-
-__global__ __launch_bounds__(256, 3) void relgate_mfma_kernel(
-        const u16* __restrict__ relWb, const float* __restrict__ relb,
-        const u16* __restrict__ W12b, const float* __restrict__ rgb,
-        const float* __restrict__ gateb,
-        const u16* __restrict__ vattW1p, const float* __restrict__ vattb1,
-        const float* __restrict__ vattW2, const float* __restrict__ vattb2,
-        u16* __restrict__ aggB, const float* __restrict__ wsum,
-        float* __restrict__ vscores) {
-    __shared__ u16 Wf[128][136];
-    __shared__ u16 Wt[128][72];
-    int tid = threadIdx.x;
-    int wv = tid >> 6, lane = tid & 63;
-    int quad = lane >> 4, l15 = lane & 15;
-    int v = blockIdx.y;
-    int row0 = blockIdx.x * 128;
-    const size_t vbase = (size_t)v * NN;
-
-    #pragma unroll
-    for (int rep = 0; rep < 8; ++rep) {
-        int flat = rep * 256 + tid;
-        int n = flat >> 4, c8 = flat & 15;
-        int gr = row0 + n; if (gr >= NN) gr = NN - 1;
-        uint4 q = *reinterpret_cast<const uint4*>(aggB + (vbase + gr) * DD + c8 * 8);
-        *reinterpret_cast<uint4*>(&Wf[n][c8 * 8]) = q;
-    }
-    __syncthreads();
-
-    s8v af[2][2][2];
-    #pragma unroll
-    for (int h = 0; h < 2; ++h)
-        #pragma unroll
-        for (int t = 0; t < 2; ++t) {
-            int kl = h * 64 + t * 32 + quad * 8;
-            af[h][t][0] = *reinterpret_cast<const s8v*>(&Wf[wv * 32 + l15][kl]);
-            af[h][t][1] = *reinterpret_cast<const s8v*>(&Wf[wv * 32 + 16 + l15][kl]);
-        }
-    __syncthreads();
-
-    const u16* W1 = relWb + (size_t)v * DD * DD;
-    const u16* W2 = W12b + (size_t)v * DD * DD;
-    #pragma unroll
-    for (int rep = 0; rep < 8; ++rep) {
-        int flat = rep * 256 + tid;
-        int n = flat >> 4, c8 = flat & 15;
-        *reinterpret_cast<uint4*>(&Wf[n][c8 * 8]) =
-            *reinterpret_cast<const uint4*>(W1 + (size_t)n * DD + c8 * 8);
-    }
-    #pragma unroll
-    for (int rep = 0; rep < 4; ++rep) {
-        int flat = rep * 256 + tid;
-        int n = flat >> 3, c8 = flat & 7;
-        *reinterpret_cast<uint4*>(&Wt[n][c8 * 8]) =
-            *reinterpret_cast<const uint4*>(W2 + (size_t)n * DD + c8 * 8);
-    }
-    __syncthreads();
-
-    f4v acc1[2][8], acc2[2][8];
-    #pragma unroll
-    for (int rt = 0; rt < 2; ++rt)
-        #pragma unroll
-        for (int c = 0; c < 8; ++c) {
-            acc1[rt][c] = f4v{0.f, 0.f, 0.f, 0.f};
-            acc2[rt][c] = f4v{0.f, 0.f, 0.f, 0.f};
-        }
-
-    #pragma unroll
-    for (int h = 0; h < 2; ++h)
-        #pragma unroll
-        for (int t = 0; t < 2; ++t) {
-            int kl = h * 64 + t * 32 + quad * 8;
-            #pragma unroll
-            for (int c = 0; c < 8; ++c) {
-                s8v b = *reinterpret_cast<const s8v*>(&Wf[c * 16 + l15][kl]);
-                acc1[0][c] = __builtin_amdgcn_mfma_f32_16x16x32_bf16(af[h][t][0], b, acc1[0][c], 0, 0, 0);
-                acc1[1][c] = __builtin_amdgcn_mfma_f32_16x16x32_bf16(af[h][t][1], b, acc1[1][c], 0, 0, 0);
-            }
-        }
-    #pragma unroll
-    for (int t = 0; t < 2; ++t) {
-        int kl = t * 32 + quad * 8;
-        #pragma unroll
-        for (int c = 0; c < 8; ++c) {
-            s8v b = *reinterpret_cast<const s8v*>(&Wt[c * 16 + l15][kl]);
-            acc2[0][c] = __builtin_amdgcn_mfma_f32_16x16x32_bf16(af[0][t][0], b, acc2[0][c], 0, 0, 0);
-            acc2[1][c] = __builtin_amdgcn_mfma_f32_16x16x32_bf16(af[0][t][1], b, acc2[1][c], 0, 0, 0);
-        }
-    }
-    __syncthreads();
-
-    #pragma unroll
-    for (int rep = 0; rep < 4; ++rep) {
-        int flat = rep * 256 + tid;
-        int n = flat >> 3, c8 = flat & 7;
-        *reinterpret_cast<uint4*>(&Wt[n][c8 * 8]) =
-            *reinterpret_cast<const uint4*>(W2 + (size_t)n * DD + 64 + c8 * 8);
-    }
-    __syncthreads();
-    #pragma unroll
-    for (int t = 0; t < 2; ++t) {
-        int kl = t * 32 + quad * 8;
-        #pragma unroll
-        for (int c = 0; c < 8; ++c) {
-            s8v b = *reinterpret_cast<const s8v*>(&Wt[c * 16 + l15][kl]);
-            acc2[0][c] = __builtin_amdgcn_mfma_f32_16x16x32_bf16(af[1][t][0], b, acc2[0][c], 0, 0, 0);
-            acc2[1][c] = __builtin_amdgcn_mfma_f32_16x16x32_bf16(af[1][t][1], b, acc2[1][c], 0, 0, 0);
-        }
-    }
-
-    float wsn[2][4];
-    #pragma unroll
-    for (int rt = 0; rt < 2; ++rt)
-        #pragma unroll
-        for (int r = 0; r < 4; ++r) {
-            int gr = row0 + wv * 32 + rt * 16 + quad * 4 + r;
-            wsn[rt][r] = wsum[vbase + (gr < NN ? gr : NN - 1)];
-        }
-    float rb[8], rg2[8], gb[8];
-    #pragma unroll
-    for (int c = 0; c < 8; ++c) {
-        int col = c * 16 + l15;
-        rb[c]  = relb[v * DD + col];
-        rg2[c] = rgb[v * DD + col];
-        gb[c]  = gateb[v * DD + col];
-    }
-    #pragma unroll
-    for (int rt = 0; rt < 2; ++rt)
-        #pragma unroll
-        for (int c = 0; c < 8; ++c)
-            #pragma unroll
-            for (int r = 0; r < 4; ++r) {
-                float a = acc1[rt][c][r] + wsn[rt][r] * rb[c];
-                float g = fsigmoid(acc2[rt][c][r] + wsn[rt][r] * rg2[c] + gb[c]);
-                Wf[wv * 32 + rt * 16 + quad * 4 + r][c * 16 + l15] = f2bf(g * a);
-            }
-    __syncthreads();
-
-    {
-        const u16* Wv = vattW1p + (size_t)v * 64 * DD;
-        #pragma unroll
-        for (int rep = 0; rep < 4; ++rep) {
-            int flat = rep * 256 + tid;
-            int n = flat >> 4, c8 = flat & 15;
-            uint4 q = *reinterpret_cast<const uint4*>(Wv + (size_t)n * DD + c8 * 8);
-            int half = c8 >> 3;
-            *reinterpret_cast<uint4*>(&Wt[half * 64 + n][(c8 & 7) * 8]) = q;
-        }
-    }
-    s8v a2[2][2][2];
-    #pragma unroll
-    for (int h = 0; h < 2; ++h)
-        #pragma unroll
-        for (int t = 0; t < 2; ++t) {
-            int kl = h * 64 + t * 32 + quad * 8;
-            a2[h][t][0] = *reinterpret_cast<const s8v*>(&Wf[wv * 32 + l15][kl]);
-            a2[h][t][1] = *reinterpret_cast<const s8v*>(&Wf[wv * 32 + 16 + l15][kl]);
-        }
-    #pragma unroll
-    for (int rep = 0; rep < 8; ++rep) {
-        int flat = rep * 256 + tid;
-        int n = flat >> 4, c8 = flat & 15;
-        int gr = row0 + n;
-        if (gr < NN)
-            *reinterpret_cast<uint4*>(aggB + (vbase + gr) * DD + c8 * 8) =
-                *reinterpret_cast<const uint4*>(&Wf[n][c8 * 8]);
-    }
-    __syncthreads();
-
-    f4v acc3[2][4];
-    #pragma unroll
-    for (int rt = 0; rt < 2; ++rt)
-        #pragma unroll
-        for (int c = 0; c < 4; ++c)
-            acc3[rt][c] = f4v{0.f, 0.f, 0.f, 0.f};
-    #pragma unroll
-    for (int h = 0; h < 2; ++h)
-        #pragma unroll
-        for (int t = 0; t < 2; ++t) {
-            int kl = t * 32 + quad * 8;
-            #pragma unroll
-            for (int c = 0; c < 4; ++c) {
-                s8v b = *reinterpret_cast<const s8v*>(&Wt[h * 64 + c * 16 + l15][kl]);
-                acc3[0][c] = __builtin_amdgcn_mfma_f32_16x16x32_bf16(a2[h][t][0], b, acc3[0][c], 0, 0, 0);
-                acc3[1][c] = __builtin_amdgcn_mfma_f32_16x16x32_bf16(a2[h][t][1], b, acc3[1][c], 0, 0, 0);
-            }
-        }
-    float vb1[4], vw2[4];
-    #pragma unroll
-    for (int c = 0; c < 4; ++c) {
-        int col = c * 16 + l15;
-        vb1[c] = vattb1[col];
-        vw2[c] = vattW2[col];
-    }
-    float vb2 = vattb2[0];
-    #pragma unroll
-    for (int rt = 0; rt < 2; ++rt)
-        #pragma unroll
-        for (int r = 0; r < 4; ++r) {
-            float p = 0.f;
-            #pragma unroll
-            for (int c = 0; c < 4; ++c) {
-                float hv = acc3[rt][c][r] + vb1[c];
-                hv = hv > 0.f ? hv : 0.f;
-                p += hv * vw2[c];
-            }
-            #pragma unroll
-            for (int m = 1; m < 16; m <<= 1)
-                p += __shfl_xor(p, m);
-            int gr = row0 + wv * 32 + rt * 16 + quad * 4 + r;
-            if (l15 == 0 && gr < NN)
-                vscores[vbase + gr] = p + vb2;
-        }
 }
 
 __global__ __launch_bounds__(256) void relgate_kernel(
@@ -924,238 +1023,6 @@
     r.z = f2bf((bf2f(q0.z) * w0 + bf2f(q1.z) * w1 + bf2f(q2.z) * w2) * na);
     r.w = f2bf((bf2f(q0.w) * w0 + bf2f(q1.w) * w1 + bf2f(q2.w) * w2) * na);
     *reinterpret_cast<ushort4*>(aggB + off) = r;
-}
-
-__global__ __launch_bounds__(256, 3) void final_mfma_kernel(
-        const u16* __restrict__ featB, const u16* __restrict__ aggB,
-        const float* __restrict__ vsc, const float* __restrict__ natt,
-        const u16* __restrict__ WsfB, const u16* __restrict__ featWB,
-        const u16* __restrict__ fusWbB,
-        const float* __restrict__ c1, const float* __restrict__ featb,
-        const float* __restrict__ ln_g, const float* __restrict__ ln_b,
-        float* __restrict__ outp) {
-    __shared__ u16 Wf[128][136];
-    __shared__ u16 Wt[128][72];
-    int tid = threadIdx.x;
-    int wv = tid >> 6, lane = tid & 63;
-    int quad = lane >> 4, l15 = lane & 15;
-    int row0 = blockIdx.x * 128;
-
-    #pragma unroll
-    for (int rep = 0; rep < 8; ++rep) {
-        int flat = rep * 256 + tid;
-        int n = flat >> 4, c8 = flat & 15;
-        int gr = row0 + n; if (gr >= NN) gr = NN - 1;
-        uint4 q = *reinterpret_cast<const uint4*>(featB + (size_t)gr * DD + c8 * 8);
-        *reinterpret_cast<uint4*>(&Wf[n][c8 * 8]) = q;
-    }
-    if (tid < 128) {
-        int gr = row0 + tid; if (gr >= NN) gr = NN - 1;
-        float s0 = vsc[gr], s1 = vsc[NN + gr], s2 = vsc[2 * NN + gr];
-        float m = fmaxf(s0, fmaxf(s1, s2));
-        const float L2E = 1.4426950408889634f;
-        float e0 = fexp2((s0 - m) * L2E);
-        float e1 = fexp2((s1 - m) * L2E);
-        float e2 = fexp2((s2 - m) * L2E);
-        float na = natt[gr] * frcp(e0 + e1 + e2);
-        float* rwp = reinterpret_cast<float*>(&Wf[tid][128]);
-        rwp[0] = e0 * na;
-        rwp[1] = e1 * na;
-        rwp[2] = e2 * na;
-    }
-    __syncthreads();
-
-    s8v af[2][2][2];
-    #pragma unroll
-    for (int h = 0; h < 2; ++h)
-        #pragma unroll
-        for (int t = 0; t < 2; ++t) {
-            int kl = h * 64 + t * 32 + quad * 8;
-            af[h][t][0] = *reinterpret_cast<const s8v*>(&Wf[wv * 32 + l15][kl]);
-            af[h][t][1] = *reinterpret_cast<const s8v*>(&Wf[wv * 32 + 16 + l15][kl]);
-        }
-    __syncthreads();
-
-    #pragma unroll
-    for (int rep = 0; rep < 8; ++rep) {
-        int flat = rep * 256 + tid;
-        int n = flat >> 4, c8 = flat & 15;
-        *reinterpret_cast<uint4*>(&Wf[n][c8 * 8]) =
-            *reinterpret_cast<const uint4*>(WsfB + (size_t)n * DD + c8 * 8);
-    }
-    #pragma unroll
-    for (int rep = 0; rep < 4; ++rep) {
-        int flat = rep * 256 + tid;
-        int n = flat >> 3, c8 = flat & 7;
-        *reinterpret_cast<uint4*>(&Wt[n][c8 * 8]) =
-            *reinterpret_cast<const uint4*>(featWB + (size_t)n * DD + c8 * 8);
-    }
-    __syncthreads();
-
-    f4v acc1[2][8], acc2[2][8];
-    #pragma unroll
-    for (int rt = 0; rt < 2; ++rt)
-        #pragma unroll
-        for (int c = 0; c < 8; ++c) {
-            acc1[rt][c] = f4v{0.f, 0.f, 0.f, 0.f};
-            acc2[rt][c] = f4v{0.f, 0.f, 0.f, 0.f};
-        }
-
-    #pragma unroll
-    for (int h = 0; h < 2; ++h)
-        #pragma unroll
-        for (int t = 0; t < 2; ++t) {
-            int kl = h * 64 + t * 32 + quad * 8;
-            #pragma unroll
-            for (int c = 0; c < 8; ++c) {
-                s8v b = *reinterpret_cast<const s8v*>(&Wf[c * 16 + l15][kl]);
-                acc1[0][c] = __builtin_amdgcn_mfma_f32_16x16x32_bf16(af[h][t][0], b, acc1[0][c], 0, 0, 0);
-                acc1[1][c] = __builtin_amdgcn_mfma_f32_16x16x32_bf16(af[h][t][1], b, acc1[1][c], 0, 0, 0);
-            }
-        }
-    #pragma unroll
-    for (int t = 0; t < 2; ++t) {
-        int kl = t * 32 + quad * 8;
-        #pragma unroll
-        for (int c = 0; c < 8; ++c) {
-            s8v b = *reinterpret_cast<const s8v*>(&Wt[c * 16 + l15][kl]);
-            acc2[0][c] = __builtin_amdgcn_mfma_f32_16x16x32_bf16(af[0][t][0], b, acc2[0][c], 0, 0, 0);
-            acc2[1][c] = __builtin_amdgcn_mfma_f32_16x16x32_bf16(af[0][t][1], b, acc2[1][c], 0, 0, 0);
-        }
-    }
-    __syncthreads();
-    #pragma unroll
-    for (int rep = 0; rep < 4; ++rep) {
-        int flat = rep * 256 + tid;
-        int n = flat >> 3, c8 = flat & 7;
-        *reinterpret_cast<uint4*>(&Wt[n][c8 * 8]) =
-            *reinterpret_cast<const uint4*>(featWB + (size_t)n * DD + 64 + c8 * 8);
-    }
-    __syncthreads();
-    #pragma unroll
-    for (int t = 0; t < 2; ++t) {
-        int kl = t * 32 + quad * 8;
-        #pragma unroll
-        for (int c = 0; c < 8; ++c) {
-            s8v b = *reinterpret_cast<const s8v*>(&Wt[c * 16 + l15][kl]);
-            acc2[0][c] = __builtin_amdgcn_mfma_f32_16x16x32_bf16(af[1][t][0], b, acc2[0][c], 0, 0, 0);
-            acc2[1][c] = __builtin_amdgcn_mfma_f32_16x16x32_bf16(af[1][t][1], b, acc2[1][c], 0, 0, 0);
-        }
-    }
-
-    #pragma unroll
-    for (int rep = 0; rep < 8; ++rep) {
-        int flat = rep * 256 + tid;
-        int n = flat >> 4, c8 = flat & 15;
-        int gr = row0 + n; if (gr >= NN) gr = NN - 1;
-        size_t off = (size_t)gr * DD + c8 * 8;
-        uint4 q0 = *reinterpret_cast<const uint4*>(aggB + off);
-        uint4 q1 = *reinterpret_cast<const uint4*>(aggB + (size_t)NN * DD + off);
-        uint4 q2 = *reinterpret_cast<const uint4*>(aggB + 2 * (size_t)NN * DD + off);
-        const float* rwp = reinterpret_cast<const float*>(&Wf[n][128]);
-        float w0 = rwp[0], w1 = rwp[1], w2 = rwp[2];
-        u32 o[4];
-        const u32* a = &q0.x; const u32* b = &q1.x; const u32* c = &q2.x;
-        #pragma unroll
-        for (int j = 0; j < 4; ++j) {
-            float lo = bf2f((u16)(a[j] & 0xffffu)) * w0 + bf2f((u16)(b[j] & 0xffffu)) * w1
-                     + bf2f((u16)(c[j] & 0xffffu)) * w2;
-            float hi = bf2f((u16)(a[j] >> 16)) * w0 + bf2f((u16)(b[j] >> 16)) * w1
-                     + bf2f((u16)(c[j] >> 16)) * w2;
-            o[j] = (u32)f2bf(lo) | ((u32)f2bf(hi) << 16);
-        }
-        uint4 r; r.x = o[0]; r.y = o[1]; r.z = o[2]; r.w = o[3];
-        *reinterpret_cast<uint4*>(&Wf[n][c8 * 8]) = r;
-    }
-    __syncthreads();
-
-    #pragma unroll
-    for (int rep = 0; rep < 4; ++rep) {
-        int flat = rep * 256 + tid;
-        int n = flat >> 3, c8 = flat & 7;
-        *reinterpret_cast<uint4*>(&Wt[n][c8 * 8]) =
-            *reinterpret_cast<const uint4*>(fusWbB + (size_t)n * DD + c8 * 8);
-    }
-    __syncthreads();
-    #pragma unroll
-    for (int t = 0; t < 2; ++t) {
-        int kl = t * 32 + quad * 8;
-        s8v a0 = *reinterpret_cast<const s8v*>(&Wf[wv * 32 + l15][kl]);
-        s8v a1 = *reinterpret_cast<const s8v*>(&Wf[wv * 32 + 16 + l15][kl]);
-        #pragma unroll
-        for (int c = 0; c < 8; ++c) {
-            s8v b = *reinterpret_cast<const s8v*>(&Wt[c * 16 + l15][kl]);
-            acc1[0][c] = __builtin_amdgcn_mfma_f32_16x16x32_bf16(a0, b, acc1[0][c], 0, 0, 0);
-            acc1[1][c] = __builtin_amdgcn_mfma_f32_16x16x32_bf16(a1, b, acc1[1][c], 0, 0, 0);
-        }
-    }
-    __syncthreads();
-    #pragma unroll
-    for (int rep = 0; rep < 4; ++rep) {
-        int flat = rep * 256 + tid;
-        int n = flat >> 3, c8 = flat & 7;
-        *reinterpret_cast<uint4*>(&Wt[n][c8 * 8]) =
-            *reinterpret_cast<const uint4*>(fusWbB + (size_t)n * DD + 64 + c8 * 8);
-    }
-    __syncthreads();
-    #pragma unroll
-    for (int t = 0; t < 2; ++t) {
-        int kl = t * 32 + quad * 8;
-        s8v a0 = *reinterpret_cast<const s8v*>(&Wf[wv * 32 + l15][64 + kl]);
-        s8v a1 = *reinterpret_cast<const s8v*>(&Wf[wv * 32 + 16 + l15][64 + kl]);
-        #pragma unroll
-        for (int c = 0; c < 8; ++c) {
-            s8v b = *reinterpret_cast<const s8v*>(&Wt[c * 16 + l15][kl]);
-            acc1[0][c] = __builtin_amdgcn_mfma_f32_16x16x32_bf16(a0, b, acc1[0][c], 0, 0, 0);
-            acc1[1][c] = __builtin_amdgcn_mfma_f32_16x16x32_bf16(a1, b, acc1[1][c], 0, 0, 0);
-        }
-    }
-
-    float c1j[8], fbj[8], gj[8], bj[8];
-    #pragma unroll
-    for (int c = 0; c < 8; ++c) {
-        int col = c * 16 + l15;
-        c1j[c] = c1[col];
-        fbj[c] = featb[col];
-        gj[c]  = ln_g[col];
-        bj[c]  = ln_b[col];
-    }
-    #pragma unroll
-    for (int rt = 0; rt < 2; ++rt)
-        #pragma unroll
-        for (int c = 0; c < 8; ++c)
-            #pragma unroll
-            for (int r = 0; r < 4; ++r) {
-                float f = acc1[rt][c][r] + c1j[c];
-                f = f > 0.f ? f : 0.f;
-                acc1[rt][c][r] = f + acc2[rt][c][r] + fbj[c];
-            }
-    #pragma unroll
-    for (int rt = 0; rt < 2; ++rt)
-        #pragma unroll
-        for (int r = 0; r < 4; ++r) {
-            float s = 0.f, q = 0.f;
-            #pragma unroll
-            for (int c = 0; c < 8; ++c) {
-                float x = acc1[rt][c][r];
-                s += x; q += x * x;
-            }
-            #pragma unroll
-            for (int m = 1; m < 16; m <<= 1) {
-                s += __shfl_xor(s, m);
-                q += __shfl_xor(q, m);
-            }
-            float mu = s * (1.f / 128.f);
-            float var = q * (1.f / 128.f) - mu * mu;
-            float rs = rsqrtf(var + 1e-5f);
-            int gr = row0 + wv * 32 + rt * 16 + quad * 4 + r;
-            if (gr < NN) {
-                #pragma unroll
-                for (int c = 0; c < 8; ++c)
-                    outp[(size_t)gr * DD + c * 16 + l15] =
-                        (acc1[rt][c][r] - mu) * rs * gj[c] + bj[c];
-            }
-        }
 }
 
 __global__ __launch_bounds__(256) void final_kernel(
@@ -1309,8 +1176,6 @@
         wprep3_kernel<<<128, 128, 0, stream>>>(attW1, attW1B);
         wprep4_kernel<<<192, 128, 0, stream>>>(vattW1, view_pref, vattW1p);
         wprep5_kernel<<<VV * 129, 128, 0, stream>>>(relW, gateW, relb, W12b, rgb);
-        label_mfma_kernel<<<RGB, 256, 0, stream>>>(featB, attW1B, clsW, clsb, attb1,
-                                                   attW2, attb2, att_bias, natt, probs);
         hipMemsetAsync(C, 0, (size_t)TOT * sizeof(int), stream);
         count_kernel<<<(VV * EE + 255) / 256, 256, 0, stream>>>(edst, C);
         scanA_kernel<<<NB, 256, 0, stream>>>(C, bs);
@@ -1318,12 +1183,11 @@
         scanC_kernel<<<NB, 256, 0, stream>>>(C, bs);
         fill_kernel<<<(VV * EE + 255) / 256, 256, 0, stream>>>(esrc, edst, ew, C, bsw);
         gather_kernel<<<(VV * NN) / 4, 256, 0, stream>>>(featB, C, bsw, aggB, wsum);
-        relgate_mfma_kernel<<<dim3(RGB, 3), 256, 0, stream>>>(relWb, relb, W12b, rgb, gateb,
-                                                              vattW1p, vattb1, vattW2, vattb2,
-                                                              aggB, wsum, vsc);
-        final_mfma_kernel<<<RGB, 256, 0, stream>>>(featB, aggB, vsc, natt,
-                                                   WsfB, featWB, fusWbB,
-                                                   c1, featb, ln_g, ln_b, outp);
+        fused_mfma_kernel<<<RGB, 256, 0, stream>>>(
+            featB, aggB, attW1B, clsW, clsb, attb1, attW2, attb2, att_bias,
+            relWb, relb, W12b, rgb, gateb,
+            vattW1p, vattb1, vattW2, vattb2, wsum,
+            WsfB, featWB, fusWbB, c1, featb, ln_g, ln_b, outp, probs);
     } else {
         label_kernel<<<3125, 256, 0, stream>>>(feat, clsW, clsb, attW1, attb1, attW2, attb2,
                                                att_bias, natt, probs);
```

After: 715.4 us. +8.2%, slower.
